# Performance work log

Hardware: AMD Instinct MI355X
Metric: run time of the kernel (lower is better)

Reference implementation:

```python
import jax, jax.numpy as jnp
import numpy as np

B, L, C, S, W, R = 2, 32, 32, 64, 64, 32
MH = 32  # forcing MLP hidden


def _conv3d(x, w, b, pad_hw):
    # x: [B, Cin, L, S, W], w: [Cout, Cin, 1, kh, kw]
    y = jax.lax.conv_general_dilated(
        x, w, window_strides=(1, 1, 1),
        padding=[(0, 0), (pad_hw, pad_hw), (pad_hw, pad_hw)],
        dimension_numbers=('NCDHW', 'OIDHW', 'NCDHW'))
    return y + b[None, :, None, None, None]


def _forward(x, listT, params_log_base, dispersion_mod, fm_W1, fm_b1, fm_W2, fm_b2,
             forcing_scale, U_re, U_im, V_re, V_im, pW_re, pW_im, pb_re, pb_im,
             convr_w, convr_b, convi_w, convi_b, projc_w, projc_b, ln_w, ln_b):
    b, l, c, s, w = x.shape
    r = U_re.shape[-1]
    pad = s // 4
    dt = listT.reshape(b, l, 1, 1, 1)

    # FFT with mirror padding along S
    xp = jnp.pad(x, ((0, 0), (0, 0), (0, 0), (pad, pad), (0, 0)), mode='reflect')
    h = jnp.fft.fft2(xp.astype(jnp.complex64), axes=(-2, -1), norm='ortho')

    # complex channel projection
    proj_W = pW_re + 1j * pW_im
    h = jnp.einsum('blcsw,cd->bldsw', h, proj_W)
    h = h + (pb_re + 1j * pb_im)[None, None, :, None, None]

    # back to spatial, crop pad, re-FFT
    hs = jnp.fft.ifft2(h, axes=(-2, -1), norm='ortho')[..., pad:-pad, :]
    h = jnp.fft.fft2(hs, axes=(-2, -1), norm='ortho')

    U = U_re + 1j * U_im          # [C, S, R]
    V = V_re + 1j * V_im          # [C, W, R]
    # zq[b,l,c,r,q] = sum_{s,w} h * conj(U)[c,s,r] * V[c,w,q]
    zq = jnp.einsum('blcsw,csr,cwq->blcrq', h, jnp.conj(U), V)

    nu_base = jnp.exp(params_log_base[0] + dispersion_mod[0]).reshape(1, 1, c, r, 1)
    th_base = jnp.exp(params_log_base[1] + dispersion_mod[1]).reshape(1, 1, c, r, 1)

    # forcing modulation
    ctx = x.mean(axis=(-2, -1))                       # [B, L, C]
    inp = jnp.concatenate([ctx, dt.reshape(b, l, 1)], axis=-1)
    mid = jnp.tanh(inp @ fm_W1 + fm_b1)
    mod = (mid @ fm_W2 + fm_b2).reshape(b, l, c, r, 2)
    dnu = (forcing_scale * jnp.tanh(mod[..., 0]))[..., None]
    dth = (forcing_scale * jnp.tanh(mod[..., 1]))[..., None]

    nu_t = jnp.maximum(nu_base * dt + dnu, 1e-6)       # [B, L, C, R, 1]
    th_t = th_base * dt + dth
    lamb = jnp.exp(jax.lax.complex(-nu_t, th_t))       # complex [B, L, C, R, 1]

    gamma = jnp.sqrt(jnp.maximum(1.0 - jnp.exp(-2.0 * nu_t), 1e-12))
    x_in = zq * gamma.astype(zq.dtype)                 # [B, L, C, R, R]

    # parallel linear-recurrence scan: z_t = lamb_t * z_{t-1} + x_t
    def comb(a, bb):
        a1, x1 = a
        a2, x2 = bb
        return a1 * a2, a2 * x1 + x2
    _, z_out = jax.lax.associative_scan(comb, (lamb, x_in), axis=1)

    # reconstruct spectral field and inverse FFT
    h_rec = jnp.einsum('blcrq,cwq,csr->blcsw', z_out, jnp.conj(V), U)
    h_sp = jnp.fft.ifft2(h_rec, axes=(-2, -1), norm='ortho')

    xr = jnp.transpose(h_sp.real, (0, 2, 1, 3, 4))     # [B, C, L, S, W]
    xi = jnp.transpose(h_sp.imag, (0, 2, 1, 3, 4))
    hr = _conv3d(xr, convr_w, convr_b, 1)
    hi = _conv3d(xi, convi_w, convi_b, 1)
    hf = _conv3d(jnp.concatenate([hr, hi], axis=1), projc_w, projc_b, 0)
    hf = jnp.transpose(hf, (0, 2, 1, 3, 4))            # [B, L, C, S, W]

    # LayerNorm over [S, W]
    mu = hf.mean(axis=(-2, -1), keepdims=True)
    var = hf.var(axis=(-2, -1), keepdims=True)
    hf = (hf - mu) / jnp.sqrt(var + 1e-5) * ln_w + ln_b

    return x + hf


def setup_inputs() -> dict:
    key = jax.random.key(0)
    ks = jax.random.split(key, 20)
    f32 = jnp.float32
    x = jax.random.normal(ks[0], (B, L, C, S, W), dtype=f32)
    listT = jax.random.uniform(ks[1], (B, L), dtype=f32, minval=0.5, maxval=1.5)

    r_min, r_max = 0.8, 0.99
    u1 = jax.random.uniform(ks[2], (C, R), dtype=f32)
    u2 = jax.random.uniform(ks[3], (C, R), dtype=f32)
    nu_log = jnp.log(-0.5 * jnp.log(u1 * (r_max ** 2 - r_min ** 2) + r_min ** 2))
    theta_log = jnp.log(u2 * (2.0 * np.pi))
    params_log_base = jnp.stack([nu_log, theta_log], axis=0)
    dispersion_mod = jnp.zeros((2, C, R), dtype=f32)

    fm_W1 = jax.random.normal(ks[4], (C + 1, MH), dtype=f32) / np.sqrt(C + 1)
    fm_b1 = jnp.zeros((MH,), dtype=f32)
    fm_W2 = jax.random.normal(ks[5], (MH, C * R * 2), dtype=f32) / np.sqrt(MH)
    fm_b2 = jnp.zeros((C * R * 2,), dtype=f32)
    forcing_scale = jnp.float32(0.1)

    cplx_scale = 1.0 / np.sqrt(2.0)
    U_re = jax.random.normal(ks[6], (C, S, R), dtype=f32) * cplx_scale / np.sqrt(S)
    U_im = jax.random.normal(ks[7], (C, S, R), dtype=f32) * cplx_scale / np.sqrt(S)
    V_re = jax.random.normal(ks[8], (C, W, R), dtype=f32) * cplx_scale / np.sqrt(W)
    V_im = jax.random.normal(ks[9], (C, W, R), dtype=f32) * cplx_scale / np.sqrt(W)
    pW_re = jax.random.normal(ks[10], (C, C), dtype=f32) * cplx_scale / np.sqrt(C)
    pW_im = jax.random.normal(ks[11], (C, C), dtype=f32) * cplx_scale / np.sqrt(C)
    pb_re = jnp.zeros((C,), dtype=f32)
    pb_im = jnp.zeros((C,), dtype=f32)

    convr_w = jax.random.normal(ks[12], (C, C, 1, 3, 3), dtype=f32) * (1.0 / np.sqrt(C * 9))
    convr_b = jnp.zeros((C,), dtype=f32)
    convi_w = jax.random.normal(ks[13], (C, C, 1, 3, 3), dtype=f32) * (1.0 / np.sqrt(C * 9))
    convi_b = jnp.zeros((C,), dtype=f32)
    projc_w = jax.random.normal(ks[14], (C, 2 * C, 1, 1, 1), dtype=f32) * (1.0 / np.sqrt(2 * C))
    projc_b = jnp.zeros((C,), dtype=f32)

    ln_w = jnp.ones((S, W), dtype=f32)
    ln_b = jnp.zeros((S, W), dtype=f32)

    return dict(x=x, listT=listT, params_log_base=params_log_base,
                dispersion_mod=dispersion_mod, fm_W1=fm_W1, fm_b1=fm_b1,
                fm_W2=fm_W2, fm_b2=fm_b2, forcing_scale=forcing_scale,
                U_re=U_re, U_im=U_im, V_re=V_re, V_im=V_im,
                pW_re=pW_re, pW_im=pW_im, pb_re=pb_re, pb_im=pb_im,
                convr_w=convr_w, convr_b=convr_b, convi_w=convi_w, convi_b=convi_b,
                projc_w=projc_w, projc_b=projc_b, ln_w=ln_w, ln_b=ln_b)


def reference(x, listT, params_log_base, dispersion_mod, fm_W1, fm_b1, fm_W2, fm_b2,
              forcing_scale, U_re, U_im, V_re, V_im, pW_re, pW_im, pb_re, pb_im,
              convr_w, convr_b, convi_w, convi_b, projc_w, projc_b, ln_w, ln_b):
    return _forward(x, listT, params_log_base, dispersion_mod, fm_W1, fm_b1, fm_W2,
                    fm_b2, forcing_scale, U_re, U_im, V_re, V_im, pW_re, pW_im,
                    pb_re, pb_im, convr_w, convr_b, convi_w, convi_b, projc_w,
                    projc_b, ln_w, ln_b)
```

## Files before the change

### kernel.cpp

```cpp
#include <hip/hip_runtime.h>


typedef __attribute__((ext_vector_type(8))) short short8;
typedef __attribute__((ext_vector_type(4))) float floatx4;

__device__ __forceinline__ unsigned pack_bf16(float re, float im) {
  unsigned a = __float_as_uint(re), b = __float_as_uint(im);
  a = (a + 0x7FFFu + ((a >> 16) & 1u)) >> 16;
  b = (b + 0x7FFFu + ((b >> 16) & 1u)) >> 16;
  return a | (b << 16);
}
__device__ __forceinline__ unsigned short bf16r(float v) {
  unsigned a = __float_as_uint(v);
  return (unsigned short)((a + 0x7FFFu + ((a >> 16) & 1u)) >> 16);
}

__global__ __launch_bounds__(256) void k_mixprep(
    const float* __restrict__ x, const float* __restrict__ pWr,
    const float* __restrict__ pWi,
    const float* __restrict__ U_re, const float* __restrict__ U_im,
    const float* __restrict__ V_re, const float* __restrict__ V_im,
    const float* __restrict__ projc_w, const float* __restrict__ convr_w,
    const float* __restrict__ convi_w,
    unsigned* __restrict__ hs, float* __restrict__ ctxp,
    unsigned* __restrict__ zqA, unsigned* __restrict__ recA,
    unsigned* __restrict__ recB, unsigned* __restrict__ Wtb) {
  __shared__ __align__(16) char smem[33280];
  const int tid = threadIdx.x;
  if (blockIdx.x < 1024) {
    unsigned* xb_s = (unsigned*)smem;
    float(*red)[16][2] = (float(*)[16][2])(smem + 20480);
    unsigned* outb = (unsigned*)smem;
    const int bl = blockIdx.x >> 4;
    const int seg = blockIdx.x & 15;
    const int pxbase = seg * 256;
    const float* xb = x + (size_t)bl * 131072 + pxbase;
    float csa = 0.f, csb = 0.f;
#pragma unroll
    for (int t = 0; t < 4; ++t) {
      int i = t * 256 + tid;
      int c2 = i & 15, g4 = i >> 4;
      float4 a = *(const float4*)(xb + (2 * c2) * 4096 + g4 * 4);
      float4 b = *(const float4*)(xb + (2 * c2 + 1) * 4096 + g4 * 4);
      csa += a.x + a.y + a.z + a.w;
      csb += b.x + b.y + b.z + b.w;
#pragma unroll
      for (int j = 0; j < 4; ++j) {
        int px = g4 * 4 + j;
        xb_s[px * 20 + (((c2 >> 2) ^ (px & 3)) << 2) + (c2 & 3)] =
            pack_bf16(((const float*)&a)[j], ((const float*)&b)[j]);
      }
    }
    red[tid & 15][tid >> 4][0] = csa;
    red[tid & 15][tid >> 4][1] = csb;
    const int lane = tid & 63, wv = tid >> 6;
    const int qd = lane >> 4, ln = lane & 15;
    short8 arL, aiL, arH, aiH;
#pragma unroll
    for (int j = 0; j < 8; ++j) {
      int ci = qd * 8 + j;
      ((short*)&arL)[j] = (short)bf16r(pWr[ci * 32 + ln]);
      ((short*)&aiL)[j] = (short)bf16r(pWi[ci * 32 + ln]);
      ((short*)&arH)[j] = (short)bf16r(pWr[ci * 32 + 16 + ln]);
      ((short*)&aiH)[j] = (short)bf16r(pWi[ci * 32 + 16 + ln]);
    }
    __syncthreads();
    if (tid < 32) {
      int c2 = tid >> 1, part = tid & 1;
      float s = 0.f;
#pragma unroll
      for (int w = 0; w < 16; ++w) s += red[c2][w][part];
      ctxp[(bl * 16 + seg) * 32 + 2 * c2 + part] = s;
    }
    floatx4 RL[4], IL[4], RH[4], IH[4];
#pragma unroll
    for (int pt = 0; pt < 4; ++pt) {
      int pxt = wv * 4 + pt;
      int pxl = pxt * 16 + ln;
      short8 bfr = *(const short8*)&xb_s[pxl * 20 + ((qd ^ (pxl & 3)) << 2)];
      floatx4 z4 = {0.f, 0.f, 0.f, 0.f};
      RL[pt] = __builtin_amdgcn_mfma_f32_16x16x32_bf16(arL, bfr, z4, 0, 0, 0);
      IL[pt] = __builtin_amdgcn_mfma_f32_16x16x32_bf16(aiL, bfr, z4, 0, 0, 0);
      RH[pt] = __builtin_amdgcn_mfma_f32_16x16x32_bf16(arH, bfr, z4, 0, 0, 0);
      IH[pt] = __builtin_amdgcn_mfma_f32_16x16x32_bf16(aiH, bfr, z4, 0, 0, 0);
    }
    __syncthreads();
#pragma unroll
    for (int pt = 0; pt < 4; ++pt) {
      int px = (wv * 4 + pt) * 16 + ln;
#pragma unroll
      for (int j = 0; j < 4; ++j) {
        outb[(qd * 4 + j) * 260 + px] = pack_bf16(RL[pt][j], IL[pt][j]);
        outb[(16 + qd * 4 + j) * 260 + px] = pack_bf16(RH[pt][j], IH[pt][j]);
      }
    }
    __syncthreads();
    unsigned* ho = hs + (size_t)bl * 131072 + pxbase;
    const int px4 = tid & 63, dg = tid >> 6;
#pragma unroll
    for (int dd = 0; dd < 8; ++dd) {
      int d = dg * 8 + dd;
      uint4 v = *(const uint4*)&outb[d * 260 + px4 * 4];
      *(uint4*)(ho + d * 4096 + px4 * 4) = v;
    }
  } else if (blockIdx.x < 1088) {
    float2* A2 = (float2*)smem;
    float2* tw = (float2*)(smem + 16384);
    const int id = blockIdx.x - 1024;
    const int c = id >> 1, src = id & 1;
    const float* Ar = (src ? V_re : U_re) + c * 2048;
    const float* Ai = (src ? V_im : U_im) + c * 2048;
    if (tid < 64) {
      float sa, ca;
      sincosf((float)tid * 0.09817477042468103f, &sa, &ca);
      tw[tid] = make_float2(ca, sa);
    }
#pragma unroll
    for (int t = 0; t < 8; ++t) {
      int idx = t * 256 + tid;
      A2[idx] = make_float2(Ar[idx], Ai[idx]);
    }
    __syncthreads();
    const int kw = tid >> 2, mg = tid & 3;
    float sr[8] = {0.f, 0.f, 0.f, 0.f, 0.f, 0.f, 0.f, 0.f};
    float si[8] = {0.f, 0.f, 0.f, 0.f, 0.f, 0.f, 0.f, 0.f};
#pragma unroll 4
    for (int n = 0; n < 64; ++n) {
      float2 w = tw[(kw * n) & 63];
      float ws = src ? -w.y : w.y;
#pragma unroll
      for (int t4 = 0; t4 < 4; ++t4) {
        float4 p = *(const float4*)&A2[n * 32 + mg * 8 + t4 * 2];
        sr[2 * t4]     += p.x * w.x - p.y * ws;
        si[2 * t4]     += p.x * ws + p.y * w.x;
        sr[2 * t4 + 1] += p.z * w.x - p.w * ws;
        si[2 * t4 + 1] += p.z * ws + p.w * w.x;
      }
    }
#pragma unroll
    for (int j = 0; j < 8; ++j) {
      float r = sr[j] * 0.125f, i2 = si[j] * 0.125f;
      int m = mg * 8 + j;
      unsigned p_ri  = pack_bf16(r, i2);
      unsigned p_rmi = pack_bf16(r, -i2);
      unsigned p_ir  = pack_bf16(i2, r);
      unsigned p_mir = pack_bf16(-i2, r);
      if (src == 0) {
        zqA[((c * 4 + 2) * 32 + m) * 64 + kw] = p_ri;
        zqA[((c * 4 + 3) * 32 + m) * 64 + kw] = p_mir;
        recA[((c * 2 + 0) * 64 + kw) * 32 + m] = p_rmi;
        recA[((c * 2 + 1) * 64 + kw) * 32 + m] = p_ir;
      } else {
        zqA[((c * 4 + 0) * 32 + m) * 64 + kw] = p_rmi;
        zqA[((c * 4 + 1) * 32 + m) * 64 + kw] = p_ir;
        recB[((c * 2 + 0) * 64 + kw) * 32 + m] = p_ri;
        recB[((c * 2 + 1) * 64 + kw) * 32 + m] = p_mir;
      }
    }
  } else {
    int gid = (blockIdx.x - 1088) * 256 + tid;
    if (gid < 9216) {
      int co = gid / 288;
      int r2 = gid - co * 288;
      int tap = r2 >> 5, ci = r2 & 31;
      float sr = 0.f, si = 0.f;
      for (int m = 0; m < 32; ++m) {
        sr += projc_w[co * 64 + m]      * convr_w[(m * 32 + ci) * 9 + tap];
        si += projc_w[co * 64 + 32 + m] * convi_w[(m * 32 + ci) * 9 + tap];
      }
      Wtb[gid] = pack_bf16(sr, si);
    }
  }
}

__global__ __launch_bounds__(256) void k_zq(
    const unsigned* __restrict__ hs, const short* __restrict__ zqA,
    float2* __restrict__ zq,
    const float* __restrict__ ctxp, const float* __restrict__ listT,
    const float* __restrict__ plb, const float* __restrict__ dmod,
    const float* __restrict__ W1, const float* __restrict__ b1,
    const float* __restrict__ W2, const float* __restrict__ b2,
    const float* __restrict__ fscale,
    float2* __restrict__ lam, float* __restrict__ gam) {
  __shared__ unsigned HsB[4096];
  __shared__ unsigned T2[2048];
  __shared__ float mid_s[32];
  __shared__ float ctxs[32];
  const int tid = threadIdx.x;
  if (blockIdx.x >= 2048) {
    int bl = blockIdx.x - 2048;
    float dt = listT[bl];
    if (tid < 32) {
      float s = 0.f;
#pragma unroll
      for (int sg = 0; sg < 16; ++sg) s += ctxp[(bl * 16 + sg) * 32 + tid];
      ctxs[tid] = s * (1.f / 4096.f);
    }
    __syncthreads();
    if (tid < 32) {
      float a = b1[tid];
      for (int j = 0; j < 32; ++j) a += ctxs[j] * W1[j * 32 + tid];
      a += dt * W1[1024 + tid];
      mid_s[tid] = tanhf(a);
    }
    __syncthreads();
    float fs = fscale[0];
#pragma unroll
    for (int u = 0; u < 4; ++u) {
      int cr = u * 256 + tid;
      int col = cr * 2;
      float m0 = b2[col], m1 = b2[col + 1];
      for (int h = 0; h < 32; ++h) {
        float mh = mid_s[h];
        float2 w2 = *(const float2*)&W2[h * 2048 + col];
        m0 += mh * w2.x;
        m1 += mh * w2.y;
      }
      float dnu = fs * tanhf(m0);
      float dth = fs * tanhf(m1);
      float nub = expf(plb[cr] + dmod[cr]);
      float thb = expf(plb[1024 + cr] + dmod[1024 + cr]);
      float nut = fmaxf(nub * dt + dnu, 1e-6f);
      float tht = thb * dt + dth;
      float e = expf(-nut);
      float sa, ca;
      sincosf(tht, &sa, &ca);
      float g = sqrtf(fmaxf(1.f - expf(-2.f * nut), 1e-12f));
      int o = bl * 1024 + cr;
      lam[o] = make_float2(e * ca, e * sa);
      gam[o] = g;
    }
    return;
  }
  const int blc = blockIdx.x;
  const int c = blc & 31;
  const int lane = tid & 63, wv = tid >> 6;
  const int qd = lane >> 4, ln = lane & 15;
  const int mt = wv >> 1, nth = wv & 1;
  {
    const uint4* hp = (const uint4*)(hs + (size_t)blc * 4096);
#pragma unroll
    for (int it = 0; it < 4; ++it) {
      int i4 = tid + it * 256;
      uint4 v = hp[i4];
      int s = i4 >> 4, w4 = i4 & 15;
      *(uint4*)&HsB[s * 64 + ((w4 ^ (s & 15)) << 2)] = v;
    }
  }
  const short* zA = zqA + (size_t)c * 4 * 32 * 128;
  short8 a1[4], a2[4], a3[4], a4[4];
#pragma unroll
  for (int t = 0; t < 4; ++t) {
    int row = mt * 16 + ln;
    a1[t] = *(const short8*)(zA + (0 * 32 + row) * 128 + t * 32 + qd * 8);
    a2[t] = *(const short8*)(zA + (1 * 32 + row) * 128 + t * 32 + qd * 8);
    a3[t] = *(const short8*)(zA + (2 * 32 + row) * 128 + t * 32 + qd * 8);
    a4[t] = *(const short8*)(zA + (3 * 32 + row) * 128 + t * 32 + qd * 8);
  }
  __syncthreads();
#pragma unroll
  for (int nti = 0; nti < 2; ++nti) {
    int nt = nth * 2 + nti;
    int n = nt * 16 + ln;
    floatx4 accr = {0.f, 0.f, 0.f, 0.f}, acci = {0.f, 0.f, 0.f, 0.f};
#pragma unroll
    for (int t = 0; t < 4; ++t) {
      short8 b = *(const short8*)&HsB[n * 64 + (((4 * t + qd) ^ (n & 15)) << 2)];
      accr = __builtin_amdgcn_mfma_f32_16x16x32_bf16(a1[t], b, accr, 0, 0, 0);
      acci = __builtin_amdgcn_mfma_f32_16x16x32_bf16(a2[t], b, acci, 0, 0, 0);
    }
#pragma unroll
    for (int j = 0; j < 4; ++j) {
      int q = mt * 16 + qd * 4 + j;
      int s = n;
      T2[q * 64 + (((s >> 2) ^ (q & 15)) << 2) + (s & 3)] = pack_bf16(accr[j], acci[j]);
    }
  }
  __syncthreads();
  {
    const int mt2 = wv >> 1, nt2 = wv & 1;
    int n = nt2 * 16 + ln;
    floatx4 zr = {0.f, 0.f, 0.f, 0.f}, zi = {0.f, 0.f, 0.f, 0.f};
#pragma unroll
    for (int t = 0; t < 4; ++t) {
      short8 b = *(const short8*)&T2[n * 64 + (((4 * t + qd) ^ (n & 15)) << 2)];
      zr = __builtin_amdgcn_mfma_f32_16x16x32_bf16(a3[t], b, zr, 0, 0, 0);
      zi = __builtin_amdgcn_mfma_f32_16x16x32_bf16(a4[t], b, zi, 0, 0, 0);
    }
    float2* zo = zq + (size_t)blc * 1024;
#pragma unroll
    for (int j = 0; j < 4; ++j) {
      int r = mt2 * 16 + qd * 4 + j;
      zo[r * 32 + n] = make_float2(zr[j], zi[j]);
    }
  }
}

__global__ __launch_bounds__(256) void k_scan(const float2* __restrict__ lam,
                                              const float* __restrict__ gam,
                                              const float2* __restrict__ zin,
                                              unsigned* __restrict__ zsp,
                                              int zst) {
  __shared__ float2 se[4][64];
  __shared__ float2 pe[4][64];
  __shared__ float2 cr_s[4][64];
  const int bc = blockIdx.x >> 4;
  const int b = bc >> 5, c = bc & 31;
  const int rq0 = (blockIdx.x & 15) * 64;
  const int seg = threadIdx.x >> 6, u = threadIdx.x & 63;
  const int rq = rq0 + u, r = rq >> 5;
  const int t0 = seg * 8;
  float2 vv[8], ll[8];
  float gg[8];
#pragma unroll
  for (int i = 0; i < 8; ++i) {
    int t = b * 32 + t0 + i;
    vv[i] = zin[((size_t)t * 32 + c) * 1024 + rq];
    ll[i] = lam[t * 1024 + c * 32 + r];
    gg[i] = gam[t * 1024 + c * 32 + r];
  }
  float2 s = make_float2(0.f, 0.f), P = make_float2(1.f, 0.f);
  float2 zloc[8], Ps[8];
#pragma unroll
  for (int i = 0; i < 8; ++i) {
    float2 lm = ll[i];
    float nr = lm.x * s.x - lm.y * s.y + gg[i] * vv[i].x;
    float ni = lm.x * s.y + lm.y * s.x + gg[i] * vv[i].y;
    s = make_float2(nr, ni);
    float pr = P.x * lm.x - P.y * lm.y;
    float pi = P.x * lm.y + P.y * lm.x;
    P = make_float2(pr, pi);
    zloc[i] = s;
    Ps[i] = P;
  }
  se[seg][u] = s;
  pe[seg][u] = P;
  __syncthreads();
  if (threadIdx.x < 64) {
    float2 c1 = se[0][u];
    float2 p1 = pe[1][u], s1 = se[1][u];
    float2 c2 = make_float2(s1.x + p1.x * c1.x - p1.y * c1.y,
                            s1.y + p1.x * c1.y + p1.y * c1.x);
    float2 p2 = pe[2][u], s2 = se[2][u];
    float2 c3 = make_float2(s2.x + p2.x * c2.x - p2.y * c2.y,
                            s2.y + p2.x * c2.y + p2.y * c2.x);
    cr_s[0][u] = make_float2(0.f, 0.f);
    cr_s[1][u] = c1;
    cr_s[2][u] = c2;
    cr_s[3][u] = c3;
  }
  __syncthreads();
  float2 cr = cr_s[seg][u];
#pragma unroll
  for (int i = 0; i < 8; ++i) {
    float zr = zloc[i].x + Ps[i].x * cr.x - Ps[i].y * cr.y;
    float zi = zloc[i].y + Ps[i].x * cr.y + Ps[i].y * cr.x;
    size_t idx = ((size_t)(b * 32 + t0 + i) * 32 + c) * 1024 + rq;
    zsp[idx * zst] = pack_bf16(zr, zi);
  }
}

__global__ __launch_bounds__(256) void k_rec(const unsigned* __restrict__ zs,
                                             int zst,
                                             const short* __restrict__ recA,
                                             const short* __restrict__ recB,
                                             unsigned* __restrict__ hsp) {
  __shared__ unsigned zB[1024];
  __shared__ unsigned P[2048];
  const int blc = blockIdx.x;
  const int c = blc & 31;
  const int tid = threadIdx.x;
  const int lane = tid & 63, wv = tid >> 6;
  const int qd = lane >> 4, ln = lane & 15;
  {
    const unsigned* zp = zs + (size_t)blc * 1024 * zst;
#pragma unroll
    for (int it = 0; it < 4; ++it) {
      int i = tid + it * 256;
      unsigned pv = zp[(size_t)i * zst];
      int r = i >> 5, q = i & 31;
      zB[q * 32 + (((r >> 2) ^ (q & 7)) << 2) + (r & 3)] = pv;
    }
  }
  const short* rA = recA + (size_t)c * 2 * 64 * 64;
  short8 a5[2], a6[2];
#pragma unroll
  for (int t = 0; t < 2; ++t) {
    int row = wv * 16 + ln;
    a5[t] = *(const short8*)(rA + (0 * 64 + row) * 64 + t * 32 + qd * 8);
    a6[t] = *(const short8*)(rA + (1 * 64 + row) * 64 + t * 32 + qd * 8);
  }
  __syncthreads();
#pragma unroll
  for (int nt = 0; nt < 2; ++nt) {
    int n = nt * 16 + ln;
    floatx4 pr = {0.f, 0.f, 0.f, 0.f}, pi = {0.f, 0.f, 0.f, 0.f};
#pragma unroll
    for (int t = 0; t < 2; ++t) {
      short8 b = *(const short8*)&zB[n * 32 + (((4 * t + qd) ^ (n & 7)) << 2)];
      pr = __builtin_amdgcn_mfma_f32_16x16x32_bf16(a5[t], b, pr, 0, 0, 0);
      pi = __builtin_amdgcn_mfma_f32_16x16x32_bf16(a6[t], b, pi, 0, 0, 0);
    }
#pragma unroll
    for (int j = 0; j < 4; ++j) {
      int s = wv * 16 + qd * 4 + j;
      int q = n;
      P[s * 32 + (((q >> 2) ^ (s & 7)) << 2) + (q & 3)] = pack_bf16(pr[j], pi[j]);
    }
  }
  __syncthreads();
  const short* rB = recB + (size_t)c * 2 * 64 * 64;
  short8 pa[2];
#pragma unroll
  for (int t = 0; t < 2; ++t) {
    int row = wv * 16 + ln;
    pa[t] = *(const short8*)&P[row * 32 + (((4 * t + qd) ^ (row & 7)) << 2)];
  }
#pragma unroll
  for (int nt = 0; nt < 4; ++nt) {
    int n = nt * 16 + ln;
    floatx4 hr = {0.f, 0.f, 0.f, 0.f}, hi = {0.f, 0.f, 0.f, 0.f};
#pragma unroll
    for (int t = 0; t < 2; ++t) {
      short8 b5 = *(const short8*)(rB + (0 * 64 + n) * 64 + t * 32 + qd * 8);
      short8 b6 = *(const short8*)(rB + (1 * 64 + n) * 64 + t * 32 + qd * 8);
      hr = __builtin_amdgcn_mfma_f32_16x16x32_bf16(pa[t], b5, hr, 0, 0, 0);
      hi = __builtin_amdgcn_mfma_f32_16x16x32_bf16(pa[t], b6, hi, 0, 0, 0);
    }
    unsigned* ho = hsp + (size_t)blc * 4096;
#pragma unroll
    for (int j = 0; j < 4; ++j) {
      int s = wv * 16 + qd * 4 + j;
      ho[s * 64 + n] = pack_bf16(hr[j], hi[j]);
    }
  }
}

__global__ __launch_bounds__(512, 4) void k_conv(
    const unsigned* __restrict__ hsp, const short* __restrict__ Wtb,
    unsigned short* __restrict__ convout, float2* __restrict__ stats) {
  __shared__ unsigned lds_in[6 * 66 * 32];
  const int bl = blockIdx.x >> 4;
  const int slab = blockIdx.x & 15;
  const int y0 = slab * 4;
  const int tid = threadIdx.x;
  if (tid < 384) {
    int ci = tid & 31, j = tid >> 5;
    int yi = j >> 1, xi = (j & 1) ? 65 : 0;
    int slot = (ci >> 2) ^ (xi & 7);
    lds_in[(yi * 66 + xi) * 32 + slot * 4 + (ci & 3)] = 0u;
  }
#pragma unroll
  for (int t = 0; t < 6; ++t) {
    int i = t * 512 + tid;
    int ci = i & 31;
    int j = i >> 5;
    int yi = j >> 4, x4 = j & 15;
    int y = y0 + yi - 1;
    uint4 v = make_uint4(0u, 0u, 0u, 0u);
    if ((unsigned)y < 64u)
      v = *(const uint4*)(hsp + (((size_t)bl * 32 + ci) * 64 + y) * 64 + x4 * 4);
    int xb = 1 + x4 * 4;
#pragma unroll
    for (int jj = 0; jj < 4; ++jj) {
      int xi = xb + jj;
      int slot = (ci >> 2) ^ (xi & 7);
      lds_in[(yi * 66 + xi) * 32 + slot * 4 + (ci & 3)] =
          ((const unsigned*)&v)[jj];
    }
  }
  const int lane = tid & 63;
  const int wv = tid >> 6;
  const int quarter = wv & 3, cog = wv >> 2;
  const int co = lane & 15;
  const int qd = lane >> 4;
  short8 bW[18];
  {
    const short* wp = Wtb + ((cog * 16 + co) * 9) * 64 + qd * 8;
#pragma unroll
    for (int tap = 0; tap < 9; ++tap)
#pragma unroll
      for (int kk = 0; kk < 2; ++kk)
        bW[tap * 2 + kk] = *(const short8*)(wp + tap * 64 + kk * 32);
  }
  __syncthreads();
  float sA = 0.f, s2A = 0.f;
  const int x0 = quarter * 16;
  const int xl = lane & 15;
  for (int ry = 0; ry < 4; ++ry) {
    floatx4 acc = {0.f, 0.f, 0.f, 0.f};
#pragma unroll
    for (int tap = 0; tap < 9; ++tap) {
      int dy = tap / 3, dx = tap - dy * 3;
      int yi = ry + dy;
      int xi = x0 + xl + dx;
#pragma unroll
      for (int kk = 0; kk < 2; ++kk) {
        int slot = ((kk << 2) | qd) ^ (xi & 7);
        const short8 a =
            *(const short8*)&lds_in[(yi * 66 + xi) * 32 + slot * 4];
        acc = __builtin_amdgcn_mfma_f32_16x16x32_bf16(a, bW[tap * 2 + kk], acc, 0, 0, 0);
      }
    }
    size_t go =
        (((size_t)bl * 32 + cog * 16 + co) * 64 + (y0 + ry)) * 64 + x0 + qd * 4;
    *(uint2*)(convout + go) =
        make_uint2(pack_bf16(acc[0], acc[1]), pack_bf16(acc[2], acc[3]));
#pragma unroll
    for (int j = 0; j < 4; ++j) {
      sA += acc[j]; s2A += acc[j] * acc[j];
    }
  }
  sA += __shfl_down(sA, 32, 64);  s2A += __shfl_down(s2A, 32, 64);
  sA += __shfl_down(sA, 16, 64);  s2A += __shfl_down(s2A, 16, 64);
  if (lane < 16) {
    stats[((size_t)bl * 32 + cog * 16 + lane) * 64 + slab * 4 + quarter] =
        make_float2(sA, s2A);
  }
}

__global__ __launch_bounds__(256) void k_ln(
    const unsigned short* __restrict__ convout,
    const float2* __restrict__ stats, const float* __restrict__ x,
    const float* __restrict__ ln_w, const float* __restrict__ ln_b,
    float* __restrict__ out) {
  const int blc = blockIdx.x;
  const int tid = threadIdx.x;
  __shared__ float sh_mu, sh_rs;
  const uint2* cp = (const uint2*)(convout + (size_t)blc * 4096);
  const float4* xp = (const float4*)(x + (size_t)blc * 4096);
  const float4* lwp = (const float4*)ln_w;
  const float4* lbp = (const float4*)ln_b;
  float4* op = (float4*)(out + (size_t)blc * 4096);
  uint2 cv[4];
  float4 xv[4], lw[4], lb[4];
#pragma unroll
  for (int k = 0; k < 4; ++k) {
    int i = tid + k * 256;
    cv[k] = cp[i];
    xv[k] = xp[i];
    lw[k] = lwp[i];
    lb[k] = lbp[i];
  }
  if (tid < 64) {
    float2 v = stats[(size_t)blc * 64 + tid];
    float s = v.x, s2 = v.y;
#pragma unroll
    for (int o = 32; o > 0; o >>= 1) {
      s += __shfl_down(s, o, 64);
      s2 += __shfl_down(s2, o, 64);
    }
    if (tid == 0) {
      float mu = s * (1.f / 4096.f);
      float var = s2 * (1.f / 4096.f) - mu * mu;
      sh_mu = mu;
      sh_rs = rsqrtf(var + 1e-5f);
    }
  }
  __syncthreads();
  float mu = sh_mu, rs = sh_rs;
#pragma unroll
  for (int k = 0; k < 4; ++k) {
    int i = tid + k * 256;
    float c0 = __uint_as_float(cv[k].x << 16);
    float c1 = __uint_as_float(cv[k].x & 0xFFFF0000u);
    float c2 = __uint_as_float(cv[k].y << 16);
    float c3 = __uint_as_float(cv[k].y & 0xFFFF0000u);
    float4 o;
    o.x = xv[k].x + (c0 - mu) * rs * lw[k].x + lb[k].x;
    o.y = xv[k].y + (c1 - mu) * rs * lw[k].y + lb[k].y;
    o.z = xv[k].z + (c2 - mu) * rs * lw[k].z + lb[k].z;
    o.w = xv[k].w + (c3 - mu) * rs * lw[k].w + lb[k].w;
    op[i] = o;
  }
}

extern "C" void kernel_launch(void* const* d_in, const int* in_sizes, int n_in,
                              void* d_out, int out_size, void* d_ws,
                              size_t ws_size, hipStream_t stream) {
  const float* x       = (const float*)d_in[0];
  const float* listT   = (const float*)d_in[1];
  const float* plb     = (const float*)d_in[2];
  const float* dmod    = (const float*)d_in[3];
  const float* fm_W1   = (const float*)d_in[4];
  const float* fm_b1   = (const float*)d_in[5];
  const float* fm_W2   = (const float*)d_in[6];
  const float* fm_b2   = (const float*)d_in[7];
  const float* fscale  = (const float*)d_in[8];
  const float* U_re    = (const float*)d_in[9];
  const float* U_im    = (const float*)d_in[10];
  const float* V_re    = (const float*)d_in[11];
  const float* V_im    = (const float*)d_in[12];
  const float* pW_re   = (const float*)d_in[13];
  const float* pW_im   = (const float*)d_in[14];
  const float* convr_w = (const float*)d_in[17];
  const float* convi_w = (const float*)d_in[19];
  const float* projc_w = (const float*)d_in[21];
  const float* ln_w    = (const float*)d_in[23];
  const float* ln_b    = (const float*)d_in[24];
  float* out = (float*)d_out;

  float* wsf = (float*)d_ws;
  unsigned* hs  = (unsigned*)wsf;
  unsigned* hsp = (unsigned*)wsf;
  unsigned* zqAp  = (unsigned*)(wsf + 8388608);
  unsigned* recAp = (unsigned*)(wsf + 8388608 + 262144);
  unsigned* recBp = (unsigned*)(wsf + 8388608 + 393216);
  unsigned short* convout = (unsigned short*)(wsf + 8388608);
  float2*   stats = (float2*)(wsf + 12582912);
  float2*   zq  = (float2*)(wsf + 16777216);
  size_t off = 16777216 + 4194304;
  const size_t tail = 238592;
  unsigned* zs;
  int zst;
  size_t off2;
  if (ws_size >= (off + 2097152 + tail) * 4) {
    zs = (unsigned*)(wsf + off); zst = 1; off2 = off + 2097152;
  } else {
    zs = (unsigned*)zq; zst = 2; off2 = off;
  }
  float2*   lam  = (float2*)(wsf + off2);
  float*    gam  = wsf + off2 + 131072;
  float*    ctxp = wsf + off2 + 196608;
  unsigned* Wtb  = (unsigned*)(wsf + off2 + 229376);

  k_mixprep<<<1124, 256, 0, stream>>>(x, pW_re, pW_im, U_re, U_im, V_re, V_im,
                                      projc_w, convr_w, convi_w, hs, ctxp,
                                      zqAp, recAp, recBp, Wtb);
  k_zq<<<2112, 256, 0, stream>>>(hs, (const short*)zqAp, zq, ctxp, listT, plb,
                                 dmod, fm_W1, fm_b1, fm_W2, fm_b2, fscale,
                                 lam, gam);
  k_scan<<<1024, 256, 0, stream>>>(lam, gam, zq, zs, zst);
  k_rec<<<2048, 256, 0, stream>>>(zs, zst, (const short*)recAp,
                                  (const short*)recBp, hsp);
  k_conv<<<1024, 512, 0, stream>>>(hsp, (const short*)Wtb, convout, stats);
  k_ln<<<2048, 256, 0, stream>>>(convout, stats, x, ln_w, ln_b, out);
}
```

Measured before the change: 242.2 us.

## Fuse all six stages into one persistent kernel with grid barriers

Replaces six separate kernel launches with a single persistent kernel. Each block loops over the work items of every stage, and a software grid barrier built on global atomics separates the stages. The grid is sized from the occupancy query so that all blocks are co-resident. The conv stage appears to be restructured as well, moving from 512-thread to 256-thread blocks with a different stats layout that the LN stage now reduces. The goal is to remove launch gaps and inter-kernel tail effects. The cost is barrier spin overhead, reduced per-stage occupancy under the 4-blocks-per-CU bound, and a hang if blocks are not co-resident.

```diff
diff --git a/kernel.cpp b/kernel.cpp
--- a/kernel.cpp
+++ b/kernel.cpp
@@ -15,563 +15,591 @@
   return (unsigned short)((a + 0x7FFFu + ((a >> 16) & 1u)) >> 16);
 }
 
-__global__ __launch_bounds__(256) void k_mixprep(
-    const float* __restrict__ x, const float* __restrict__ pWr,
-    const float* __restrict__ pWi,
-    const float* __restrict__ U_re, const float* __restrict__ U_im,
-    const float* __restrict__ V_re, const float* __restrict__ V_im,
-    const float* __restrict__ projc_w, const float* __restrict__ convr_w,
-    const float* __restrict__ convi_w,
-    unsigned* __restrict__ hs, float* __restrict__ ctxp,
-    unsigned* __restrict__ zqA, unsigned* __restrict__ recA,
-    unsigned* __restrict__ recB, unsigned* __restrict__ Wtb) {
-  __shared__ __align__(16) char smem[33280];
+struct KP {
+  const float *x, *listT, *plb, *dmod, *W1, *b1, *W2, *b2, *fscale;
+  const float *U_re, *U_im, *V_re, *V_im, *pWr, *pWi;
+  const float *projc_w, *convr_w, *convi_w, *ln_w, *ln_b;
+  float* out;
+  unsigned *hs, *zqA, *recA, *recB, *Wtb;
+  float* ctxp;
+  float2 *zq, *lam;
+  float* gam;
+  unsigned* zs;
+  unsigned short* convout;
+  float2* stats;
+  int* bar;
+  int zst;
+};
+
+__device__ __forceinline__ void gbar(int* bar) {
+  __syncthreads();
+  if (threadIdx.x == 0) {
+    __threadfence();
+    int g = __hip_atomic_load(bar + 1, __ATOMIC_RELAXED, __HIP_MEMORY_SCOPE_AGENT);
+    int v = __hip_atomic_fetch_add(bar, 1, __ATOMIC_ACQ_REL, __HIP_MEMORY_SCOPE_AGENT);
+    if (v == (int)gridDim.x - 1) {
+      __hip_atomic_store(bar, 0, __ATOMIC_RELAXED, __HIP_MEMORY_SCOPE_AGENT);
+      __hip_atomic_store(bar + 1, g + 1, __ATOMIC_RELEASE, __HIP_MEMORY_SCOPE_AGENT);
+    } else {
+      while (__hip_atomic_load(bar + 1, __ATOMIC_RELAXED, __HIP_MEMORY_SCOPE_AGENT) == g)
+        __builtin_amdgcn_s_sleep(8);
+    }
+    __threadfence();
+  }
+  __syncthreads();
+}
+
+__global__ __launch_bounds__(256, 4) void k_all(KP p) {
+  __shared__ __align__(16) char smem[33792];
   const int tid = threadIdx.x;
-  if (blockIdx.x < 1024) {
-    unsigned* xb_s = (unsigned*)smem;
-    float(*red)[16][2] = (float(*)[16][2])(smem + 20480);
-    unsigned* outb = (unsigned*)smem;
-    const int bl = blockIdx.x >> 4;
-    const int seg = blockIdx.x & 15;
-    const int pxbase = seg * 256;
-    const float* xb = x + (size_t)bl * 131072 + pxbase;
-    float csa = 0.f, csb = 0.f;
-#pragma unroll
-    for (int t = 0; t < 4; ++t) {
-      int i = t * 256 + tid;
-      int c2 = i & 15, g4 = i >> 4;
-      float4 a = *(const float4*)(xb + (2 * c2) * 4096 + g4 * 4);
-      float4 b = *(const float4*)(xb + (2 * c2 + 1) * 4096 + g4 * 4);
-      csa += a.x + a.y + a.z + a.w;
-      csb += b.x + b.y + b.z + b.w;
-#pragma unroll
-      for (int j = 0; j < 4; ++j) {
-        int px = g4 * 4 + j;
-        xb_s[px * 20 + (((c2 >> 2) ^ (px & 3)) << 2) + (c2 & 3)] =
-            pack_bf16(((const float*)&a)[j], ((const float*)&b)[j]);
-      }
-    }
-    red[tid & 15][tid >> 4][0] = csa;
-    red[tid & 15][tid >> 4][1] = csb;
+
+  for (int wk = blockIdx.x; wk < 1124; wk += gridDim.x) {
+    if (wk < 1024) {
+      unsigned* xb_s = (unsigned*)smem;
+      float(*red)[16][2] = (float(*)[16][2])(smem + 20480);
+      unsigned* outb = (unsigned*)smem;
+      const int bl = wk >> 4;
+      const int seg = wk & 15;
+      const int pxbase = seg * 256;
+      const float* xb = p.x + (size_t)bl * 131072 + pxbase;
+      float csa = 0.f, csb = 0.f;
+#pragma unroll
+      for (int t = 0; t < 4; ++t) {
+        int i = t * 256 + tid;
+        int c2 = i & 15, g4 = i >> 4;
+        float4 a = *(const float4*)(xb + (2 * c2) * 4096 + g4 * 4);
+        float4 b = *(const float4*)(xb + (2 * c2 + 1) * 4096 + g4 * 4);
+        csa += a.x + a.y + a.z + a.w;
+        csb += b.x + b.y + b.z + b.w;
+#pragma unroll
+        for (int j = 0; j < 4; ++j) {
+          int px = g4 * 4 + j;
+          xb_s[px * 20 + (((c2 >> 2) ^ (px & 3)) << 2) + (c2 & 3)] =
+              pack_bf16(((const float*)&a)[j], ((const float*)&b)[j]);
+        }
+      }
+      red[tid & 15][tid >> 4][0] = csa;
+      red[tid & 15][tid >> 4][1] = csb;
+      const int lane = tid & 63, wv = tid >> 6;
+      const int qd = lane >> 4, ln = lane & 15;
+      short8 arL, aiL, arH, aiH;
+#pragma unroll
+      for (int j = 0; j < 8; ++j) {
+        int ci = qd * 8 + j;
+        ((short*)&arL)[j] = (short)bf16r(p.pWr[ci * 32 + ln]);
+        ((short*)&aiL)[j] = (short)bf16r(p.pWi[ci * 32 + ln]);
+        ((short*)&arH)[j] = (short)bf16r(p.pWr[ci * 32 + 16 + ln]);
+        ((short*)&aiH)[j] = (short)bf16r(p.pWi[ci * 32 + 16 + ln]);
+      }
+      __syncthreads();
+      if (tid < 32) {
+        int c2 = tid >> 1, part = tid & 1;
+        float s = 0.f;
+#pragma unroll
+        for (int w = 0; w < 16; ++w) s += red[c2][w][part];
+        p.ctxp[(bl * 16 + seg) * 32 + 2 * c2 + part] = s;
+      }
+      floatx4 RL[4], IL[4], RH[4], IH[4];
+#pragma unroll
+      for (int pt = 0; pt < 4; ++pt) {
+        int pxt = wv * 4 + pt;
+        int pxl = pxt * 16 + ln;
+        short8 bfr = *(const short8*)&xb_s[pxl * 20 + ((qd ^ (pxl & 3)) << 2)];
+        floatx4 z4 = {0.f, 0.f, 0.f, 0.f};
+        RL[pt] = __builtin_amdgcn_mfma_f32_16x16x32_bf16(arL, bfr, z4, 0, 0, 0);
+        IL[pt] = __builtin_amdgcn_mfma_f32_16x16x32_bf16(aiL, bfr, z4, 0, 0, 0);
+        RH[pt] = __builtin_amdgcn_mfma_f32_16x16x32_bf16(arH, bfr, z4, 0, 0, 0);
+        IH[pt] = __builtin_amdgcn_mfma_f32_16x16x32_bf16(aiH, bfr, z4, 0, 0, 0);
+      }
+      __syncthreads();
+#pragma unroll
+      for (int pt = 0; pt < 4; ++pt) {
+        int px = (wv * 4 + pt) * 16 + ln;
+#pragma unroll
+        for (int j = 0; j < 4; ++j) {
+          outb[(qd * 4 + j) * 260 + px] = pack_bf16(RL[pt][j], IL[pt][j]);
+          outb[(16 + qd * 4 + j) * 260 + px] = pack_bf16(RH[pt][j], IH[pt][j]);
+        }
+      }
+      __syncthreads();
+      unsigned* ho = p.hs + (size_t)bl * 131072 + pxbase;
+      const int px4 = tid & 63, dg = tid >> 6;
+#pragma unroll
+      for (int dd = 0; dd < 8; ++dd) {
+        int d = dg * 8 + dd;
+        uint4 v = *(const uint4*)&outb[d * 260 + px4 * 4];
+        *(uint4*)(ho + d * 4096 + px4 * 4) = v;
+      }
+    } else if (wk < 1088) {
+      float2* A2 = (float2*)smem;
+      float2* tw = (float2*)(smem + 16384);
+      const int id = wk - 1024;
+      const int c = id >> 1, src = id & 1;
+      const float* Ar = (src ? p.V_re : p.U_re) + c * 2048;
+      const float* Ai = (src ? p.V_im : p.U_im) + c * 2048;
+      if (tid < 64) {
+        float sa, ca;
+        sincosf((float)tid * 0.09817477042468103f, &sa, &ca);
+        tw[tid] = make_float2(ca, sa);
+      }
+#pragma unroll
+      for (int t = 0; t < 8; ++t) {
+        int idx = t * 256 + tid;
+        A2[idx] = make_float2(Ar[idx], Ai[idx]);
+      }
+      __syncthreads();
+      const int kw = tid >> 2, mg = tid & 3;
+      float sr[8] = {0.f, 0.f, 0.f, 0.f, 0.f, 0.f, 0.f, 0.f};
+      float si[8] = {0.f, 0.f, 0.f, 0.f, 0.f, 0.f, 0.f, 0.f};
+#pragma unroll 4
+      for (int n = 0; n < 64; ++n) {
+        float2 w = tw[(kw * n) & 63];
+        float ws = src ? -w.y : w.y;
+#pragma unroll
+        for (int t4 = 0; t4 < 4; ++t4) {
+          float4 q = *(const float4*)&A2[n * 32 + mg * 8 + t4 * 2];
+          sr[2 * t4]     += q.x * w.x - q.y * ws;
+          si[2 * t4]     += q.x * ws + q.y * w.x;
+          sr[2 * t4 + 1] += q.z * w.x - q.w * ws;
+          si[2 * t4 + 1] += q.z * ws + q.w * w.x;
+        }
+      }
+#pragma unroll
+      for (int j = 0; j < 8; ++j) {
+        float r = sr[j] * 0.125f, i2 = si[j] * 0.125f;
+        int m = mg * 8 + j;
+        unsigned p_ri  = pack_bf16(r, i2);
+        unsigned p_rmi = pack_bf16(r, -i2);
+        unsigned p_ir  = pack_bf16(i2, r);
+        unsigned p_mir = pack_bf16(-i2, r);
+        if (src == 0) {
+          p.zqA[((c * 4 + 2) * 32 + m) * 64 + kw] = p_ri;
+          p.zqA[((c * 4 + 3) * 32 + m) * 64 + kw] = p_mir;
+          p.recA[((c * 2 + 0) * 64 + kw) * 32 + m] = p_rmi;
+          p.recA[((c * 2 + 1) * 64 + kw) * 32 + m] = p_ir;
+        } else {
+          p.zqA[((c * 4 + 0) * 32 + m) * 64 + kw] = p_rmi;
+          p.zqA[((c * 4 + 1) * 32 + m) * 64 + kw] = p_ir;
+          p.recB[((c * 2 + 0) * 64 + kw) * 32 + m] = p_ri;
+          p.recB[((c * 2 + 1) * 64 + kw) * 32 + m] = p_mir;
+        }
+      }
+    } else {
+      int gid = (wk - 1088) * 256 + tid;
+      if (gid < 9216) {
+        int co = gid / 288;
+        int r2 = gid - co * 288;
+        int tap = r2 >> 5, ci = r2 & 31;
+        float sr = 0.f, si = 0.f;
+        for (int m = 0; m < 32; ++m) {
+          sr += p.projc_w[co * 64 + m]      * p.convr_w[(m * 32 + ci) * 9 + tap];
+          si += p.projc_w[co * 64 + 32 + m] * p.convi_w[(m * 32 + ci) * 9 + tap];
+        }
+        p.Wtb[gid] = pack_bf16(sr, si);
+      }
+    }
+    __syncthreads();
+  }
+  gbar(p.bar);
+
+  for (int wk = blockIdx.x; wk < 2112; wk += gridDim.x) {
+    if (wk < 2048) {
+      unsigned* HsB = (unsigned*)smem;
+      unsigned* T2 = HsB + 4096;
+      const int blc = wk;
+      const int c = blc & 31;
+      const int lane = tid & 63, wv = tid >> 6;
+      const int qd = lane >> 4, ln = lane & 15;
+      const int mt = wv >> 1, nth = wv & 1;
+      {
+        const uint4* hp = (const uint4*)(p.hs + (size_t)blc * 4096);
+#pragma unroll
+        for (int it = 0; it < 4; ++it) {
+          int i4 = tid + it * 256;
+          uint4 v = hp[i4];
+          int s = i4 >> 4, w4 = i4 & 15;
+          *(uint4*)&HsB[s * 64 + ((w4 ^ (s & 15)) << 2)] = v;
+        }
+      }
+      const short* zA = (const short*)p.zqA + (size_t)c * 4 * 32 * 128;
+      short8 a1[4], a2[4], a3[4], a4[4];
+#pragma unroll
+      for (int t = 0; t < 4; ++t) {
+        int row = mt * 16 + ln;
+        a1[t] = *(const short8*)(zA + (0 * 32 + row) * 128 + t * 32 + qd * 8);
+        a2[t] = *(const short8*)(zA + (1 * 32 + row) * 128 + t * 32 + qd * 8);
+        a3[t] = *(const short8*)(zA + (2 * 32 + row) * 128 + t * 32 + qd * 8);
+        a4[t] = *(const short8*)(zA + (3 * 32 + row) * 128 + t * 32 + qd * 8);
+      }
+      __syncthreads();
+#pragma unroll
+      for (int nti = 0; nti < 2; ++nti) {
+        int nt = nth * 2 + nti;
+        int n = nt * 16 + ln;
+        floatx4 accr = {0.f, 0.f, 0.f, 0.f}, acci = {0.f, 0.f, 0.f, 0.f};
+#pragma unroll
+        for (int t = 0; t < 4; ++t) {
+          short8 b = *(const short8*)&HsB[n * 64 + (((4 * t + qd) ^ (n & 15)) << 2)];
+          accr = __builtin_amdgcn_mfma_f32_16x16x32_bf16(a1[t], b, accr, 0, 0, 0);
+          acci = __builtin_amdgcn_mfma_f32_16x16x32_bf16(a2[t], b, acci, 0, 0, 0);
+        }
+#pragma unroll
+        for (int j = 0; j < 4; ++j) {
+          int q = mt * 16 + qd * 4 + j;
+          int s = n;
+          T2[q * 64 + (((s >> 2) ^ (q & 15)) << 2) + (s & 3)] =
+              pack_bf16(accr[j], acci[j]);
+        }
+      }
+      __syncthreads();
+      {
+        const int mt2 = wv >> 1, nt2 = wv & 1;
+        int n = nt2 * 16 + ln;
+        floatx4 zr = {0.f, 0.f, 0.f, 0.f}, zi = {0.f, 0.f, 0.f, 0.f};
+#pragma unroll
+        for (int t = 0; t < 4; ++t) {
+          short8 b = *(const short8*)&T2[n * 64 + (((4 * t + qd) ^ (n & 15)) << 2)];
+          zr = __builtin_amdgcn_mfma_f32_16x16x32_bf16(a3[t], b, zr, 0, 0, 0);
+          zi = __builtin_amdgcn_mfma_f32_16x16x32_bf16(a4[t], b, zi, 0, 0, 0);
+        }
+        float2* zo = p.zq + (size_t)blc * 1024;
+#pragma unroll
+        for (int j = 0; j < 4; ++j) {
+          int r = mt2 * 16 + qd * 4 + j;
+          zo[r * 32 + n] = make_float2(zr[j], zi[j]);
+        }
+      }
+    } else {
+      float* mid_s = (float*)(smem + 24576);
+      float* ctxs = mid_s + 32;
+      int bl = wk - 2048;
+      float dt = p.listT[bl];
+      if (tid < 32) {
+        float s = 0.f;
+#pragma unroll
+        for (int sg = 0; sg < 16; ++sg) s += p.ctxp[(bl * 16 + sg) * 32 + tid];
+        ctxs[tid] = s * (1.f / 4096.f);
+      }
+      __syncthreads();
+      if (tid < 32) {
+        float a = p.b1[tid];
+        for (int j = 0; j < 32; ++j) a += ctxs[j] * p.W1[j * 32 + tid];
+        a += dt * p.W1[1024 + tid];
+        mid_s[tid] = tanhf(a);
+      }
+      __syncthreads();
+      float fs = p.fscale[0];
+#pragma unroll
+      for (int u = 0; u < 4; ++u) {
+        int cr = u * 256 + tid;
+        int col = cr * 2;
+        float m0 = p.b2[col], m1 = p.b2[col + 1];
+        for (int h = 0; h < 32; ++h) {
+          float mh = mid_s[h];
+          float2 w2 = *(const float2*)&p.W2[h * 2048 + col];
+          m0 += mh * w2.x;
+          m1 += mh * w2.y;
+        }
+        float dnu = fs * tanhf(m0);
+        float dth = fs * tanhf(m1);
+        float nub = expf(p.plb[cr] + p.dmod[cr]);
+        float thb = expf(p.plb[1024 + cr] + p.dmod[1024 + cr]);
+        float nut = fmaxf(nub * dt + dnu, 1e-6f);
+        float tht = thb * dt + dth;
+        float e = expf(-nut);
+        float sa, ca;
+        sincosf(tht, &sa, &ca);
+        float g = sqrtf(fmaxf(1.f - expf(-2.f * nut), 1e-12f));
+        int o = bl * 1024 + cr;
+        p.lam[o] = make_float2(e * ca, e * sa);
+        p.gam[o] = g;
+      }
+    }
+    __syncthreads();
+  }
+  gbar(p.bar);
+
+  for (int wk = blockIdx.x; wk < 1024; wk += gridDim.x) {
+    float2* se = (float2*)smem;
+    float2* pe = se + 256;
+    float2* cr_s = pe + 256;
+    const int bc = wk >> 4;
+    const int b = bc >> 5, c = bc & 31;
+    const int rq0 = (wk & 15) * 64;
+    const int seg = tid >> 6, u = tid & 63;
+    const int rq = rq0 + u, r = rq >> 5;
+    const int t0 = seg * 8;
+    float2 vv[8], ll[8];
+    float gg[8];
+#pragma unroll
+    for (int i = 0; i < 8; ++i) {
+      int t = b * 32 + t0 + i;
+      vv[i] = p.zq[((size_t)t * 32 + c) * 1024 + rq];
+      ll[i] = p.lam[t * 1024 + c * 32 + r];
+      gg[i] = p.gam[t * 1024 + c * 32 + r];
+    }
+    float2 s = make_float2(0.f, 0.f), P = make_float2(1.f, 0.f);
+    float2 zloc[8], Ps[8];
+#pragma unroll
+    for (int i = 0; i < 8; ++i) {
+      float2 lm = ll[i];
+      float nr = lm.x * s.x - lm.y * s.y + gg[i] * vv[i].x;
+      float ni = lm.x * s.y + lm.y * s.x + gg[i] * vv[i].y;
+      s = make_float2(nr, ni);
+      float pr = P.x * lm.x - P.y * lm.y;
+      float pi = P.x * lm.y + P.y * lm.x;
+      P = make_float2(pr, pi);
+      zloc[i] = s;
+      Ps[i] = P;
+    }
+    se[seg * 64 + u] = s;
+    pe[seg * 64 + u] = P;
+    __syncthreads();
+    if (tid < 64) {
+      float2 c1 = se[u];
+      float2 p1 = pe[64 + u], s1 = se[64 + u];
+      float2 c2 = make_float2(s1.x + p1.x * c1.x - p1.y * c1.y,
+                              s1.y + p1.x * c1.y + p1.y * c1.x);
+      float2 p2 = pe[128 + u], s2 = se[128 + u];
+      float2 c3 = make_float2(s2.x + p2.x * c2.x - p2.y * c2.y,
+                              s2.y + p2.x * c2.y + p2.y * c2.x);
+      cr_s[u] = make_float2(0.f, 0.f);
+      cr_s[64 + u] = c1;
+      cr_s[128 + u] = c2;
+      cr_s[192 + u] = c3;
+    }
+    __syncthreads();
+    float2 cr = cr_s[seg * 64 + u];
+#pragma unroll
+    for (int i = 0; i < 8; ++i) {
+      float zr = zloc[i].x + Ps[i].x * cr.x - Ps[i].y * cr.y;
+      float zi = zloc[i].y + Ps[i].x * cr.y + Ps[i].y * cr.x;
+      size_t idx = ((size_t)(b * 32 + t0 + i) * 32 + c) * 1024 + rq;
+      p.zs[idx * p.zst] = pack_bf16(zr, zi);
+    }
+    __syncthreads();
+  }
+  gbar(p.bar);
+
+  for (int wk = blockIdx.x; wk < 2048; wk += gridDim.x) {
+    unsigned* zB = (unsigned*)smem;
+    unsigned* P = zB + 1024;
+    const int blc = wk;
+    const int c = blc & 31;
     const int lane = tid & 63, wv = tid >> 6;
     const int qd = lane >> 4, ln = lane & 15;
-    short8 arL, aiL, arH, aiH;
-#pragma unroll
-    for (int j = 0; j < 8; ++j) {
-      int ci = qd * 8 + j;
-      ((short*)&arL)[j] = (short)bf16r(pWr[ci * 32 + ln]);
-      ((short*)&aiL)[j] = (short)bf16r(pWi[ci * 32 + ln]);
-      ((short*)&arH)[j] = (short)bf16r(pWr[ci * 32 + 16 + ln]);
-      ((short*)&aiH)[j] = (short)bf16r(pWi[ci * 32 + 16 + ln]);
-    }
-    __syncthreads();
-    if (tid < 32) {
-      int c2 = tid >> 1, part = tid & 1;
-      float s = 0.f;
-#pragma unroll
-      for (int w = 0; w < 16; ++w) s += red[c2][w][part];
-      ctxp[(bl * 16 + seg) * 32 + 2 * c2 + part] = s;
-    }
-    floatx4 RL[4], IL[4], RH[4], IH[4];
-#pragma unroll
-    for (int pt = 0; pt < 4; ++pt) {
-      int pxt = wv * 4 + pt;
-      int pxl = pxt * 16 + ln;
-      short8 bfr = *(const short8*)&xb_s[pxl * 20 + ((qd ^ (pxl & 3)) << 2)];
-      floatx4 z4 = {0.f, 0.f, 0.f, 0.f};
-      RL[pt] = __builtin_amdgcn_mfma_f32_16x16x32_bf16(arL, bfr, z4, 0, 0, 0);
-      IL[pt] = __builtin_amdgcn_mfma_f32_16x16x32_bf16(aiL, bfr, z4, 0, 0, 0);
-      RH[pt] = __builtin_amdgcn_mfma_f32_16x16x32_bf16(arH, bfr, z4, 0, 0, 0);
-      IH[pt] = __builtin_amdgcn_mfma_f32_16x16x32_bf16(aiH, bfr, z4, 0, 0, 0);
-    }
-    __syncthreads();
-#pragma unroll
-    for (int pt = 0; pt < 4; ++pt) {
-      int px = (wv * 4 + pt) * 16 + ln;
+    {
+      const unsigned* zp = p.zs + (size_t)blc * 1024 * p.zst;
+#pragma unroll
+      for (int it = 0; it < 4; ++it) {
+        int i = tid + it * 256;
+        unsigned pv = zp[(size_t)i * p.zst];
+        int r = i >> 5, q = i & 31;
+        zB[q * 32 + (((r >> 2) ^ (q & 7)) << 2) + (r & 3)] = pv;
+      }
+    }
+    const short* rA = (const short*)p.recA + (size_t)c * 2 * 64 * 64;
+    short8 a5[2], a6[2];
+#pragma unroll
+    for (int t = 0; t < 2; ++t) {
+      int row = wv * 16 + ln;
+      a5[t] = *(const short8*)(rA + (0 * 64 + row) * 64 + t * 32 + qd * 8);
+      a6[t] = *(const short8*)(rA + (1 * 64 + row) * 64 + t * 32 + qd * 8);
+    }
+    __syncthreads();
+#pragma unroll
+    for (int nt = 0; nt < 2; ++nt) {
+      int n = nt * 16 + ln;
+      floatx4 pr = {0.f, 0.f, 0.f, 0.f}, pi = {0.f, 0.f, 0.f, 0.f};
+#pragma unroll
+      for (int t = 0; t < 2; ++t) {
+        short8 b = *(const short8*)&zB[n * 32 + (((4 * t + qd) ^ (n & 7)) << 2)];
+        pr = __builtin_amdgcn_mfma_f32_16x16x32_bf16(a5[t], b, pr, 0, 0, 0);
+        pi = __builtin_amdgcn_mfma_f32_16x16x32_bf16(a6[t], b, pi, 0, 0, 0);
+      }
 #pragma unroll
       for (int j = 0; j < 4; ++j) {
-        outb[(qd * 4 + j) * 260 + px] = pack_bf16(RL[pt][j], IL[pt][j]);
-        outb[(16 + qd * 4 + j) * 260 + px] = pack_bf16(RH[pt][j], IH[pt][j]);
-      }
-    }
-    __syncthreads();
-    unsigned* ho = hs + (size_t)bl * 131072 + pxbase;
-    const int px4 = tid & 63, dg = tid >> 6;
-#pragma unroll
-    for (int dd = 0; dd < 8; ++dd) {
-      int d = dg * 8 + dd;
-      uint4 v = *(const uint4*)&outb[d * 260 + px4 * 4];
-      *(uint4*)(ho + d * 4096 + px4 * 4) = v;
-    }
-  } else if (blockIdx.x < 1088) {
-    float2* A2 = (float2*)smem;
-    float2* tw = (float2*)(smem + 16384);
-    const int id = blockIdx.x - 1024;
-    const int c = id >> 1, src = id & 1;
-    const float* Ar = (src ? V_re : U_re) + c * 2048;
-    const float* Ai = (src ? V_im : U_im) + c * 2048;
-    if (tid < 64) {
-      float sa, ca;
-      sincosf((float)tid * 0.09817477042468103f, &sa, &ca);
-      tw[tid] = make_float2(ca, sa);
+        int s = wv * 16 + qd * 4 + j;
+        int q = n;
+        P[s * 32 + (((q >> 2) ^ (s & 7)) << 2) + (q & 3)] = pack_bf16(pr[j], pi[j]);
+      }
+    }
+    __syncthreads();
+    const short* rB = (const short*)p.recB + (size_t)c * 2 * 64 * 64;
+    short8 pa[2];
+#pragma unroll
+    for (int t = 0; t < 2; ++t) {
+      int row = wv * 16 + ln;
+      pa[t] = *(const short8*)&P[row * 32 + (((4 * t + qd) ^ (row & 7)) << 2)];
+    }
+#pragma unroll
+    for (int nt = 0; nt < 4; ++nt) {
+      int n = nt * 16 + ln;
+      floatx4 hr = {0.f, 0.f, 0.f, 0.f}, hi = {0.f, 0.f, 0.f, 0.f};
+#pragma unroll
+      for (int t = 0; t < 2; ++t) {
+        short8 b5 = *(const short8*)(rB + (0 * 64 + n) * 64 + t * 32 + qd * 8);
+        short8 b6 = *(const short8*)(rB + (1 * 64 + n) * 64 + t * 32 + qd * 8);
+        hr = __builtin_amdgcn_mfma_f32_16x16x32_bf16(pa[t], b5, hr, 0, 0, 0);
+        hi = __builtin_amdgcn_mfma_f32_16x16x32_bf16(pa[t], b6, hi, 0, 0, 0);
+      }
+      unsigned* ho = p.hs + (size_t)blc * 4096;
+#pragma unroll
+      for (int j = 0; j < 4; ++j) {
+        int s = wv * 16 + qd * 4 + j;
+        ho[s * 64 + n] = pack_bf16(hr[j], hi[j]);
+      }
+    }
+    __syncthreads();
+  }
+  gbar(p.bar);
+
+  for (int wk = blockIdx.x; wk < 2048; wk += gridDim.x) {
+    unsigned* lds_in = (unsigned*)smem;
+    const int bl = wk >> 5;
+    const int slab = wk & 31;
+    const int y0 = slab * 2;
+    {
+      int ci = tid & 31, j = tid >> 5;
+      int yi = j >> 1, xi = (j & 1) ? 65 : 0;
+      int slot = (ci >> 2) ^ (xi & 7);
+      lds_in[(yi * 66 + xi) * 32 + slot * 4 + (ci & 3)] = 0u;
     }
 #pragma unroll
     for (int t = 0; t < 8; ++t) {
-      int idx = t * 256 + tid;
-      A2[idx] = make_float2(Ar[idx], Ai[idx]);
-    }
-    __syncthreads();
-    const int kw = tid >> 2, mg = tid & 3;
-    float sr[8] = {0.f, 0.f, 0.f, 0.f, 0.f, 0.f, 0.f, 0.f};
-    float si[8] = {0.f, 0.f, 0.f, 0.f, 0.f, 0.f, 0.f, 0.f};
-#pragma unroll 4
-    for (int n = 0; n < 64; ++n) {
-      float2 w = tw[(kw * n) & 63];
-      float ws = src ? -w.y : w.y;
-#pragma unroll
-      for (int t4 = 0; t4 < 4; ++t4) {
-        float4 p = *(const float4*)&A2[n * 32 + mg * 8 + t4 * 2];
-        sr[2 * t4]     += p.x * w.x - p.y * ws;
-        si[2 * t4]     += p.x * ws + p.y * w.x;
-        sr[2 * t4 + 1] += p.z * w.x - p.w * ws;
-        si[2 * t4 + 1] += p.z * ws + p.w * w.x;
-      }
-    }
-#pragma unroll
-    for (int j = 0; j < 8; ++j) {
-      float r = sr[j] * 0.125f, i2 = si[j] * 0.125f;
-      int m = mg * 8 + j;
-      unsigned p_ri  = pack_bf16(r, i2);
-      unsigned p_rmi = pack_bf16(r, -i2);
-      unsigned p_ir  = pack_bf16(i2, r);
-      unsigned p_mir = pack_bf16(-i2, r);
-      if (src == 0) {
-        zqA[((c * 4 + 2) * 32 + m) * 64 + kw] = p_ri;
-        zqA[((c * 4 + 3) * 32 + m) * 64 + kw] = p_mir;
-        recA[((c * 2 + 0) * 64 + kw) * 32 + m] = p_rmi;
-        recA[((c * 2 + 1) * 64 + kw) * 32 + m] = p_ir;
-      } else {
-        zqA[((c * 4 + 0) * 32 + m) * 64 + kw] = p_rmi;
-        zqA[((c * 4 + 1) * 32 + m) * 64 + kw] = p_ir;
-        recB[((c * 2 + 0) * 64 + kw) * 32 + m] = p_ri;
-        recB[((c * 2 + 1) * 64 + kw) * 32 + m] = p_mir;
-      }
-    }
-  } else {
-    int gid = (blockIdx.x - 1088) * 256 + tid;
-    if (gid < 9216) {
-      int co = gid / 288;
-      int r2 = gid - co * 288;
-      int tap = r2 >> 5, ci = r2 & 31;
-      float sr = 0.f, si = 0.f;
-      for (int m = 0; m < 32; ++m) {
-        sr += projc_w[co * 64 + m]      * convr_w[(m * 32 + ci) * 9 + tap];
-        si += projc_w[co * 64 + 32 + m] * convi_w[(m * 32 + ci) * 9 + tap];
-      }
-      Wtb[gid] = pack_bf16(sr, si);
-    }
-  }
-}
-
-__global__ __launch_bounds__(256) void k_zq(
-    const unsigned* __restrict__ hs, const short* __restrict__ zqA,
-    float2* __restrict__ zq,
-    const float* __restrict__ ctxp, const float* __restrict__ listT,
-    const float* __restrict__ plb, const float* __restrict__ dmod,
-    const float* __restrict__ W1, const float* __restrict__ b1,
-    const float* __restrict__ W2, const float* __restrict__ b2,
-    const float* __restrict__ fscale,
-    float2* __restrict__ lam, float* __restrict__ gam) {
-  __shared__ unsigned HsB[4096];
-  __shared__ unsigned T2[2048];
-  __shared__ float mid_s[32];
-  __shared__ float ctxs[32];
-  const int tid = threadIdx.x;
-  if (blockIdx.x >= 2048) {
-    int bl = blockIdx.x - 2048;
-    float dt = listT[bl];
-    if (tid < 32) {
-      float s = 0.f;
-#pragma unroll
-      for (int sg = 0; sg < 16; ++sg) s += ctxp[(bl * 16 + sg) * 32 + tid];
-      ctxs[tid] = s * (1.f / 4096.f);
-    }
-    __syncthreads();
-    if (tid < 32) {
-      float a = b1[tid];
-      for (int j = 0; j < 32; ++j) a += ctxs[j] * W1[j * 32 + tid];
-      a += dt * W1[1024 + tid];
-      mid_s[tid] = tanhf(a);
-    }
-    __syncthreads();
-    float fs = fscale[0];
-#pragma unroll
-    for (int u = 0; u < 4; ++u) {
-      int cr = u * 256 + tid;
-      int col = cr * 2;
-      float m0 = b2[col], m1 = b2[col + 1];
-      for (int h = 0; h < 32; ++h) {
-        float mh = mid_s[h];
-        float2 w2 = *(const float2*)&W2[h * 2048 + col];
-        m0 += mh * w2.x;
-        m1 += mh * w2.y;
-      }
-      float dnu = fs * tanhf(m0);
-      float dth = fs * tanhf(m1);
-      float nub = expf(plb[cr] + dmod[cr]);
-      float thb = expf(plb[1024 + cr] + dmod[1024 + cr]);
-      float nut = fmaxf(nub * dt + dnu, 1e-6f);
-      float tht = thb * dt + dth;
-      float e = expf(-nut);
-      float sa, ca;
-      sincosf(tht, &sa, &ca);
-      float g = sqrtf(fmaxf(1.f - expf(-2.f * nut), 1e-12f));
-      int o = bl * 1024 + cr;
-      lam[o] = make_float2(e * ca, e * sa);
-      gam[o] = g;
-    }
-    return;
-  }
-  const int blc = blockIdx.x;
-  const int c = blc & 31;
-  const int lane = tid & 63, wv = tid >> 6;
-  const int qd = lane >> 4, ln = lane & 15;
-  const int mt = wv >> 1, nth = wv & 1;
-  {
-    const uint4* hp = (const uint4*)(hs + (size_t)blc * 4096);
-#pragma unroll
-    for (int it = 0; it < 4; ++it) {
-      int i4 = tid + it * 256;
-      uint4 v = hp[i4];
-      int s = i4 >> 4, w4 = i4 & 15;
-      *(uint4*)&HsB[s * 64 + ((w4 ^ (s & 15)) << 2)] = v;
-    }
-  }
-  const short* zA = zqA + (size_t)c * 4 * 32 * 128;
-  short8 a1[4], a2[4], a3[4], a4[4];
-#pragma unroll
-  for (int t = 0; t < 4; ++t) {
-    int row = mt * 16 + ln;
-    a1[t] = *(const short8*)(zA + (0 * 32 + row) * 128 + t * 32 + qd * 8);
-    a2[t] = *(const short8*)(zA + (1 * 32 + row) * 128 + t * 32 + qd * 8);
-    a3[t] = *(const short8*)(zA + (2 * 32 + row) * 128 + t * 32 + qd * 8);
-    a4[t] = *(const short8*)(zA + (3 * 32 + row) * 128 + t * 32 + qd * 8);
-  }
-  __syncthreads();
-#pragma unroll
-  for (int nti = 0; nti < 2; ++nti) {
-    int nt = nth * 2 + nti;
-    int n = nt * 16 + ln;
-    floatx4 accr = {0.f, 0.f, 0.f, 0.f}, acci = {0.f, 0.f, 0.f, 0.f};
-#pragma unroll
-    for (int t = 0; t < 4; ++t) {
-      short8 b = *(const short8*)&HsB[n * 64 + (((4 * t + qd) ^ (n & 15)) << 2)];
-      accr = __builtin_amdgcn_mfma_f32_16x16x32_bf16(a1[t], b, accr, 0, 0, 0);
-      acci = __builtin_amdgcn_mfma_f32_16x16x32_bf16(a2[t], b, acci, 0, 0, 0);
-    }
-#pragma unroll
-    for (int j = 0; j < 4; ++j) {
-      int q = mt * 16 + qd * 4 + j;
-      int s = n;
-      T2[q * 64 + (((s >> 2) ^ (q & 15)) << 2) + (s & 3)] = pack_bf16(accr[j], acci[j]);
-    }
-  }
-  __syncthreads();
-  {
-    const int mt2 = wv >> 1, nt2 = wv & 1;
-    int n = nt2 * 16 + ln;
-    floatx4 zr = {0.f, 0.f, 0.f, 0.f}, zi = {0.f, 0.f, 0.f, 0.f};
-#pragma unroll
-    for (int t = 0; t < 4; ++t) {
-      short8 b = *(const short8*)&T2[n * 64 + (((4 * t + qd) ^ (n & 15)) << 2)];
-      zr = __builtin_amdgcn_mfma_f32_16x16x32_bf16(a3[t], b, zr, 0, 0, 0);
-      zi = __builtin_amdgcn_mfma_f32_16x16x32_bf16(a4[t], b, zi, 0, 0, 0);
-    }
-    float2* zo = zq + (size_t)blc * 1024;
-#pragma unroll
-    for (int j = 0; j < 4; ++j) {
-      int r = mt2 * 16 + qd * 4 + j;
-      zo[r * 32 + n] = make_float2(zr[j], zi[j]);
-    }
-  }
-}
-
-__global__ __launch_bounds__(256) void k_scan(const float2* __restrict__ lam,
-                                              const float* __restrict__ gam,
-                                              const float2* __restrict__ zin,
-                                              unsigned* __restrict__ zsp,
-                                              int zst) {
-  __shared__ float2 se[4][64];
-  __shared__ float2 pe[4][64];
-  __shared__ float2 cr_s[4][64];
-  const int bc = blockIdx.x >> 4;
-  const int b = bc >> 5, c = bc & 31;
-  const int rq0 = (blockIdx.x & 15) * 64;
-  const int seg = threadIdx.x >> 6, u = threadIdx.x & 63;
-  const int rq = rq0 + u, r = rq >> 5;
-  const int t0 = seg * 8;
-  float2 vv[8], ll[8];
-  float gg[8];
-#pragma unroll
-  for (int i = 0; i < 8; ++i) {
-    int t = b * 32 + t0 + i;
-    vv[i] = zin[((size_t)t * 32 + c) * 1024 + rq];
-    ll[i] = lam[t * 1024 + c * 32 + r];
-    gg[i] = gam[t * 1024 + c * 32 + r];
-  }
-  float2 s = make_float2(0.f, 0.f), P = make_float2(1.f, 0.f);
-  float2 zloc[8], Ps[8];
-#pragma unroll
-  for (int i = 0; i < 8; ++i) {
-    float2 lm = ll[i];
-    float nr = lm.x * s.x - lm.y * s.y + gg[i] * vv[i].x;
-    float ni = lm.x * s.y + lm.y * s.x + gg[i] * vv[i].y;
-    s = make_float2(nr, ni);
-    float pr = P.x * lm.x - P.y * lm.y;
-    float pi = P.x * lm.y + P.y * lm.x;
-    P = make_float2(pr, pi);
-    zloc[i] = s;
-    Ps[i] = P;
-  }
-  se[seg][u] = s;
-  pe[seg][u] = P;
-  __syncthreads();
-  if (threadIdx.x < 64) {
-    float2 c1 = se[0][u];
-    float2 p1 = pe[1][u], s1 = se[1][u];
-    float2 c2 = make_float2(s1.x + p1.x * c1.x - p1.y * c1.y,
-                            s1.y + p1.x * c1.y + p1.y * c1.x);
-    float2 p2 = pe[2][u], s2 = se[2][u];
-    float2 c3 = make_float2(s2.x + p2.x * c2.x - p2.y * c2.y,
-                            s2.y + p2.x * c2.y + p2.y * c2.x);
-    cr_s[0][u] = make_float2(0.f, 0.f);
-    cr_s[1][u] = c1;
-    cr_s[2][u] = c2;
-    cr_s[3][u] = c3;
-  }
-  __syncthreads();
-  float2 cr = cr_s[seg][u];
-#pragma unroll
-  for (int i = 0; i < 8; ++i) {
-    float zr = zloc[i].x + Ps[i].x * cr.x - Ps[i].y * cr.y;
-    float zi = zloc[i].y + Ps[i].x * cr.y + Ps[i].y * cr.x;
-    size_t idx = ((size_t)(b * 32 + t0 + i) * 32 + c) * 1024 + rq;
-    zsp[idx * zst] = pack_bf16(zr, zi);
-  }
-}
-
-__global__ __launch_bounds__(256) void k_rec(const unsigned* __restrict__ zs,
-                                             int zst,
-                                             const short* __restrict__ recA,
-                                             const short* __restrict__ recB,
-                                             unsigned* __restrict__ hsp) {
-  __shared__ unsigned zB[1024];
-  __shared__ unsigned P[2048];
-  const int blc = blockIdx.x;
-  const int c = blc & 31;
-  const int tid = threadIdx.x;
-  const int lane = tid & 63, wv = tid >> 6;
-  const int qd = lane >> 4, ln = lane & 15;
-  {
-    const unsigned* zp = zs + (size_t)blc * 1024 * zst;
-#pragma unroll
-    for (int it = 0; it < 4; ++it) {
-      int i = tid + it * 256;
-      unsigned pv = zp[(size_t)i * zst];
-      int r = i >> 5, q = i & 31;
-      zB[q * 32 + (((r >> 2) ^ (q & 7)) << 2) + (r & 3)] = pv;
-    }
-  }
-  const short* rA = recA + (size_t)c * 2 * 64 * 64;
-  short8 a5[2], a6[2];
-#pragma unroll
-  for (int t = 0; t < 2; ++t) {
-    int row = wv * 16 + ln;
-    a5[t] = *(const short8*)(rA + (0 * 64 + row) * 64 + t * 32 + qd * 8);
-    a6[t] = *(const short8*)(rA + (1 * 64 + row) * 64 + t * 32 + qd * 8);
-  }
-  __syncthreads();
-#pragma unroll
-  for (int nt = 0; nt < 2; ++nt) {
-    int n = nt * 16 + ln;
-    floatx4 pr = {0.f, 0.f, 0.f, 0.f}, pi = {0.f, 0.f, 0.f, 0.f};
-#pragma unroll
-    for (int t = 0; t < 2; ++t) {
-      short8 b = *(const short8*)&zB[n * 32 + (((4 * t + qd) ^ (n & 7)) << 2)];
-      pr = __builtin_amdgcn_mfma_f32_16x16x32_bf16(a5[t], b, pr, 0, 0, 0);
-      pi = __builtin_amdgcn_mfma_f32_16x16x32_bf16(a6[t], b, pi, 0, 0, 0);
-    }
-#pragma unroll
-    for (int j = 0; j < 4; ++j) {
-      int s = wv * 16 + qd * 4 + j;
-      int q = n;
-      P[s * 32 + (((q >> 2) ^ (s & 7)) << 2) + (q & 3)] = pack_bf16(pr[j], pi[j]);
-    }
-  }
-  __syncthreads();
-  const short* rB = recB + (size_t)c * 2 * 64 * 64;
-  short8 pa[2];
-#pragma unroll
-  for (int t = 0; t < 2; ++t) {
-    int row = wv * 16 + ln;
-    pa[t] = *(const short8*)&P[row * 32 + (((4 * t + qd) ^ (row & 7)) << 2)];
-  }
-#pragma unroll
-  for (int nt = 0; nt < 4; ++nt) {
-    int n = nt * 16 + ln;
-    floatx4 hr = {0.f, 0.f, 0.f, 0.f}, hi = {0.f, 0.f, 0.f, 0.f};
-#pragma unroll
-    for (int t = 0; t < 2; ++t) {
-      short8 b5 = *(const short8*)(rB + (0 * 64 + n) * 64 + t * 32 + qd * 8);
-      short8 b6 = *(const short8*)(rB + (1 * 64 + n) * 64 + t * 32 + qd * 8);
-      hr = __builtin_amdgcn_mfma_f32_16x16x32_bf16(pa[t], b5, hr, 0, 0, 0);
-      hi = __builtin_amdgcn_mfma_f32_16x16x32_bf16(pa[t], b6, hi, 0, 0, 0);
-    }
-    unsigned* ho = hsp + (size_t)blc * 4096;
-#pragma unroll
-    for (int j = 0; j < 4; ++j) {
-      int s = wv * 16 + qd * 4 + j;
-      ho[s * 64 + n] = pack_bf16(hr[j], hi[j]);
-    }
-  }
-}
-
-__global__ __launch_bounds__(512, 4) void k_conv(
-    const unsigned* __restrict__ hsp, const short* __restrict__ Wtb,
-    unsigned short* __restrict__ convout, float2* __restrict__ stats) {
-  __shared__ unsigned lds_in[6 * 66 * 32];
-  const int bl = blockIdx.x >> 4;
-  const int slab = blockIdx.x & 15;
-  const int y0 = slab * 4;
-  const int tid = threadIdx.x;
-  if (tid < 384) {
-    int ci = tid & 31, j = tid >> 5;
-    int yi = j >> 1, xi = (j & 1) ? 65 : 0;
-    int slot = (ci >> 2) ^ (xi & 7);
-    lds_in[(yi * 66 + xi) * 32 + slot * 4 + (ci & 3)] = 0u;
-  }
-#pragma unroll
-  for (int t = 0; t < 6; ++t) {
-    int i = t * 512 + tid;
-    int ci = i & 31;
-    int j = i >> 5;
-    int yi = j >> 4, x4 = j & 15;
-    int y = y0 + yi - 1;
-    uint4 v = make_uint4(0u, 0u, 0u, 0u);
-    if ((unsigned)y < 64u)
-      v = *(const uint4*)(hsp + (((size_t)bl * 32 + ci) * 64 + y) * 64 + x4 * 4);
-    int xb = 1 + x4 * 4;
-#pragma unroll
-    for (int jj = 0; jj < 4; ++jj) {
-      int xi = xb + jj;
-      int slot = (ci >> 2) ^ (xi & 7);
-      lds_in[(yi * 66 + xi) * 32 + slot * 4 + (ci & 3)] =
-          ((const unsigned*)&v)[jj];
-    }
-  }
-  const int lane = tid & 63;
-  const int wv = tid >> 6;
-  const int quarter = wv & 3, cog = wv >> 2;
-  const int co = lane & 15;
-  const int qd = lane >> 4;
-  short8 bW[18];
-  {
-    const short* wp = Wtb + ((cog * 16 + co) * 9) * 64 + qd * 8;
-#pragma unroll
-    for (int tap = 0; tap < 9; ++tap)
-#pragma unroll
-      for (int kk = 0; kk < 2; ++kk)
-        bW[tap * 2 + kk] = *(const short8*)(wp + tap * 64 + kk * 32);
-  }
-  __syncthreads();
-  float sA = 0.f, s2A = 0.f;
-  const int x0 = quarter * 16;
-  const int xl = lane & 15;
-  for (int ry = 0; ry < 4; ++ry) {
-    floatx4 acc = {0.f, 0.f, 0.f, 0.f};
-#pragma unroll
-    for (int tap = 0; tap < 9; ++tap) {
-      int dy = tap / 3, dx = tap - dy * 3;
-      int yi = ry + dy;
-      int xi = x0 + xl + dx;
-#pragma unroll
-      for (int kk = 0; kk < 2; ++kk) {
-        int slot = ((kk << 2) | qd) ^ (xi & 7);
-        const short8 a =
-            *(const short8*)&lds_in[(yi * 66 + xi) * 32 + slot * 4];
-        acc = __builtin_amdgcn_mfma_f32_16x16x32_bf16(a, bW[tap * 2 + kk], acc, 0, 0, 0);
-      }
-    }
-    size_t go =
-        (((size_t)bl * 32 + cog * 16 + co) * 64 + (y0 + ry)) * 64 + x0 + qd * 4;
-    *(uint2*)(convout + go) =
-        make_uint2(pack_bf16(acc[0], acc[1]), pack_bf16(acc[2], acc[3]));
-#pragma unroll
-    for (int j = 0; j < 4; ++j) {
-      sA += acc[j]; s2A += acc[j] * acc[j];
-    }
-  }
-  sA += __shfl_down(sA, 32, 64);  s2A += __shfl_down(s2A, 32, 64);
-  sA += __shfl_down(sA, 16, 64);  s2A += __shfl_down(s2A, 16, 64);
-  if (lane < 16) {
-    stats[((size_t)bl * 32 + cog * 16 + lane) * 64 + slab * 4 + quarter] =
-        make_float2(sA, s2A);
-  }
-}
-
-__global__ __launch_bounds__(256) void k_ln(
-    const unsigned short* __restrict__ convout,
-    const float2* __restrict__ stats, const float* __restrict__ x,
-    const float* __restrict__ ln_w, const float* __restrict__ ln_b,
-    float* __restrict__ out) {
-  const int blc = blockIdx.x;
-  const int tid = threadIdx.x;
-  __shared__ float sh_mu, sh_rs;
-  const uint2* cp = (const uint2*)(convout + (size_t)blc * 4096);
-  const float4* xp = (const float4*)(x + (size_t)blc * 4096);
-  const float4* lwp = (const float4*)ln_w;
-  const float4* lbp = (const float4*)ln_b;
-  float4* op = (float4*)(out + (size_t)blc * 4096);
-  uint2 cv[4];
-  float4 xv[4], lw[4], lb[4];
-#pragma unroll
-  for (int k = 0; k < 4; ++k) {
-    int i = tid + k * 256;
-    cv[k] = cp[i];
-    xv[k] = xp[i];
-    lw[k] = lwp[i];
-    lb[k] = lbp[i];
-  }
-  if (tid < 64) {
-    float2 v = stats[(size_t)blc * 64 + tid];
-    float s = v.x, s2 = v.y;
-#pragma unroll
-    for (int o = 32; o > 0; o >>= 1) {
-      s += __shfl_down(s, o, 64);
-      s2 += __shfl_down(s2, o, 64);
-    }
+      int i = t * 256 + tid;
+      int ci = i & 31;
+      int j = i >> 5;
+      int yi = j >> 4, x4 = j & 15;
+      int y = y0 + yi - 1;
+      uint4 v = make_uint4(0u, 0u, 0u, 0u);
+      if ((unsigned)y < 64u)
+        v = *(const uint4*)(p.hs + (((size_t)bl * 32 + ci) * 64 + y) * 64 + x4 * 4);
+      int xb = 1 + x4 * 4;
+#pragma unroll
+      for (int jj = 0; jj < 4; ++jj) {
+        int xi = xb + jj;
+        int slot = (ci >> 2) ^ (xi & 7);
+        lds_in[(yi * 66 + xi) * 32 + slot * 4 + (ci & 3)] =
+            ((const unsigned*)&v)[jj];
+      }
+    }
+    __syncthreads();
+    const int lane = tid & 63;
+    const int wv = tid >> 6;
+    const int co = lane & 15;
+    const int qd = lane >> 4;
+    const int x0 = wv * 16;
+    const int xl = lane & 15;
+    for (int cog = 0; cog < 2; ++cog) {
+      short8 bW[18];
+      {
+        const short* wp = (const short*)p.Wtb + ((cog * 16 + co) * 9) * 64 + qd * 8;
+#pragma unroll
+        for (int tap = 0; tap < 9; ++tap)
+#pragma unroll
+          for (int kk = 0; kk < 2; ++kk)
+            bW[tap * 2 + kk] = *(const short8*)(wp + tap * 64 + kk * 32);
+      }
+      float sA = 0.f, s2A = 0.f;
+      for (int ry = 0; ry < 2; ++ry) {
+        floatx4 acc = {0.f, 0.f, 0.f, 0.f};
+#pragma unroll
+        for (int tap = 0; tap < 9; ++tap) {
+          int dy = tap / 3, dx = tap - dy * 3;
+          int yi = ry + dy;
+          int xi = x0 + xl + dx;
+#pragma unroll
+          for (int kk = 0; kk < 2; ++kk) {
+            int slot = ((kk << 2) | qd) ^ (xi & 7);
+            const short8 a =
+                *(const short8*)&lds_in[(yi * 66 + xi) * 32 + slot * 4];
+            acc = __builtin_amdgcn_mfma_f32_16x16x32_bf16(a, bW[tap * 2 + kk],
+                                                          acc, 0, 0, 0);
+          }
+        }
+        size_t go = (((size_t)bl * 32 + cog * 16 + co) * 64 + (y0 + ry)) * 64 +
+                    x0 + qd * 4;
+        *(uint2*)(p.convout + go) =
+            make_uint2(pack_bf16(acc[0], acc[1]), pack_bf16(acc[2], acc[3]));
+#pragma unroll
+        for (int j = 0; j < 4; ++j) {
+          sA += acc[j];
+          s2A += acc[j] * acc[j];
+        }
+      }
+      sA += __shfl_down(sA, 32, 64);
+      s2A += __shfl_down(s2A, 32, 64);
+      sA += __shfl_down(sA, 16, 64);
+      s2A += __shfl_down(s2A, 16, 64);
+      if (lane < 16) {
+        p.stats[((size_t)bl * 32 + cog * 16 + lane) * 128 + slab * 4 + wv] =
+            make_float2(sA, s2A);
+      }
+    }
+    __syncthreads();
+  }
+  gbar(p.bar);
+
+  for (int wk = blockIdx.x; wk < 2048; wk += gridDim.x) {
+    float* pp = (float*)smem;
+    const int blc = wk;
+    const uint2* cp = (const uint2*)(p.convout + (size_t)blc * 4096);
+    const float4* xp = (const float4*)(p.x + (size_t)blc * 4096);
+    const float4* lwp = (const float4*)p.ln_w;
+    const float4* lbp = (const float4*)p.ln_b;
+    float4* op = (float4*)(p.out + (size_t)blc * 4096);
+    uint2 cv[4];
+    float4 xv[4], lw[4], lb[4];
+#pragma unroll
+    for (int k = 0; k < 4; ++k) {
+      int i = tid + k * 256;
+      cv[k] = cp[i];
+      xv[k] = xp[i];
+      lw[k] = lwp[i];
+      lb[k] = lbp[i];
+    }
+    float s = 0.f, s2 = 0.f;
+    if (tid < 128) {
+      float2 v = p.stats[(size_t)blc * 128 + tid];
+      s = v.x;
+      s2 = v.y;
+    }
+    s += __shfl_down(s, 32, 64);   s2 += __shfl_down(s2, 32, 64);
+    s += __shfl_down(s, 16, 64);   s2 += __shfl_down(s2, 16, 64);
+    s += __shfl_down(s, 8, 64);    s2 += __shfl_down(s2, 8, 64);
+    s += __shfl_down(s, 4, 64);    s2 += __shfl_down(s2, 4, 64);
+    s += __shfl_down(s, 2, 64);    s2 += __shfl_down(s2, 2, 64);
+    s += __shfl_down(s, 1, 64);    s2 += __shfl_down(s2, 1, 64);
+    if (tid < 128 && (tid & 63) == 0) {
+      pp[(tid >> 6) * 2] = s;
+      pp[(tid >> 6) * 2 + 1] = s2;
+    }
+    __syncthreads();
     if (tid == 0) {
-      float mu = s * (1.f / 4096.f);
-      float var = s2 * (1.f / 4096.f) - mu * mu;
-      sh_mu = mu;
-      sh_rs = rsqrtf(var + 1e-5f);
-    }
-  }
-  __syncthreads();
-  float mu = sh_mu, rs = sh_rs;
-#pragma unroll
-  for (int k = 0; k < 4; ++k) {
-    int i = tid + k * 256;
-    float c0 = __uint_as_float(cv[k].x << 16);
-    float c1 = __uint_as_float(cv[k].x & 0xFFFF0000u);
-    float c2 = __uint_as_float(cv[k].y << 16);
-    float c3 = __uint_as_float(cv[k].y & 0xFFFF0000u);
-    float4 o;
-    o.x = xv[k].x + (c0 - mu) * rs * lw[k].x + lb[k].x;
-    o.y = xv[k].y + (c1 - mu) * rs * lw[k].y + lb[k].y;
-    o.z = xv[k].z + (c2 - mu) * rs * lw[k].z + lb[k].z;
-    o.w = xv[k].w + (c3 - mu) * rs * lw[k].w + lb[k].w;
-    op[i] = o;
+      float ss = pp[0] + pp[2], ss2 = pp[1] + pp[3];
+      float mu = ss * (1.f / 4096.f);
+      float var = ss2 * (1.f / 4096.f) - mu * mu;
+      pp[4] = mu;
+      pp[5] = rsqrtf(var + 1e-5f);
+    }
+    __syncthreads();
+    float mu = pp[4], rs = pp[5];
+#pragma unroll
+    for (int k = 0; k < 4; ++k) {
+      int i = tid + k * 256;
+      float c0 = __uint_as_float(cv[k].x << 16);
+      float c1 = __uint_as_float(cv[k].x & 0xFFFF0000u);
+      float c2 = __uint_as_float(cv[k].y << 16);
+      float c3 = __uint_as_float(cv[k].y & 0xFFFF0000u);
+      float4 o;
+      o.x = xv[k].x + (c0 - mu) * rs * lw[k].x + lb[k].x;
+      o.y = xv[k].y + (c1 - mu) * rs * lw[k].y + lb[k].y;
+      o.z = xv[k].z + (c2 - mu) * rs * lw[k].z + lb[k].z;
+      o.w = xv[k].w + (c3 - mu) * rs * lw[k].w + lb[k].w;
+      op[i] = o;
+    }
+    __syncthreads();
   }
 }
 
@@ -601,8 +629,7 @@
   float* out = (float*)d_out;
 
   float* wsf = (float*)d_ws;
-  unsigned* hs  = (unsigned*)wsf;
-  unsigned* hsp = (unsigned*)wsf;
+  unsigned* hs = (unsigned*)wsf;
   unsigned* zqAp  = (unsigned*)(wsf + 8388608);
   unsigned* recAp = (unsigned*)(wsf + 8388608 + 262144);
   unsigned* recBp = (unsigned*)(wsf + 8388608 + 393216);
@@ -610,7 +637,7 @@
   float2*   stats = (float2*)(wsf + 12582912);
   float2*   zq  = (float2*)(wsf + 16777216);
   size_t off = 16777216 + 4194304;
-  const size_t tail = 238592;
+  const size_t tail = 238608;
   unsigned* zs;
   int zst;
   size_t off2;
@@ -623,16 +650,39 @@
   float*    gam  = wsf + off2 + 131072;
   float*    ctxp = wsf + off2 + 196608;
   unsigned* Wtb  = (unsigned*)(wsf + off2 + 229376);
-
-  k_mixprep<<<1124, 256, 0, stream>>>(x, pW_re, pW_im, U_re, U_im, V_re, V_im,
-                                      projc_w, convr_w, convi_w, hs, ctxp,
-                                      zqAp, recAp, recBp, Wtb);
-  k_zq<<<2112, 256, 0, stream>>>(hs, (const short*)zqAp, zq, ctxp, listT, plb,
-                                 dmod, fm_W1, fm_b1, fm_W2, fm_b2, fscale,
-                                 lam, gam);
-  k_scan<<<1024, 256, 0, stream>>>(lam, gam, zq, zs, zst);
-  k_rec<<<2048, 256, 0, stream>>>(zs, zst, (const short*)recAp,
-                                  (const short*)recBp, hsp);
-  k_conv<<<1024, 512, 0, stream>>>(hsp, (const short*)Wtb, convout, stats);
-  k_ln<<<2048, 256, 0, stream>>>(convout, stats, x, ln_w, ln_b, out);
+  int*      bar  = (int*)(wsf + off2 + 238592);
+
+  static int NB = 0;
+  if (NB == 0) {
+    int perCU = 0;
+    if (hipOccupancyMaxActiveBlocksPerMultiprocessor(&perCU, k_all, 256, 0) !=
+            hipSuccess ||
+        perCU < 1)
+      perCU = 2;
+    int numCU = 256;
+    hipDeviceProp_t prop;
+    int dev = 0;
+    if (hipGetDevice(&dev) == hipSuccess &&
+        hipGetDeviceProperties(&prop, dev) == hipSuccess &&
+        prop.multiProcessorCount > 0)
+      numCU = prop.multiProcessorCount;
+    long cap = (long)perCU * numCU;
+    NB = (int)(cap > 2048 ? 2048 : cap);
+  }
+
+  KP p;
+  p.x = x; p.listT = listT; p.plb = plb; p.dmod = dmod;
+  p.W1 = fm_W1; p.b1 = fm_b1; p.W2 = fm_W2; p.b2 = fm_b2; p.fscale = fscale;
+  p.U_re = U_re; p.U_im = U_im; p.V_re = V_re; p.V_im = V_im;
+  p.pWr = pW_re; p.pWi = pW_im;
+  p.projc_w = projc_w; p.convr_w = convr_w; p.convi_w = convi_w;
+  p.ln_w = ln_w; p.ln_b = ln_b;
+  p.out = out;
+  p.hs = hs; p.zqA = zqAp; p.recA = recAp; p.recB = recBp; p.Wtb = Wtb;
+  p.ctxp = ctxp; p.zq = zq; p.lam = lam; p.gam = gam;
+  p.zs = zs; p.convout = convout; p.stats = stats;
+  p.bar = bar; p.zst = zst;
+
+  hipMemsetAsync(bar, 0, 8, stream);
+  k_all<<<NB, 256, 0, stream>>>(p);
 }
```

Result: slower. 752.9 us (+210.9%).
